# Kernel optimization log

Measured on AMD Instinct MI355X. Metric: run time of the kernel, lower is better.

The kernel has to match this reference:

```python
import jax, jax.numpy as jnp
import numpy as np

D = 256; NH = 8; HD = D // NH; FF = 1024; NLAYERS = 6
REG_MAX = 32; NBIN = REG_MAX + 1; NC = 80; KQ = 4
SPATIAL = [(80, 80), (40, 40), (20, 20)]; NPTS = [4, 4, 4]; SUMP = sum(NPTS)
LQ = 300; B = 16; OFFSET_SCALE = 0.5; UP = 0.5; REG_SCALE = 4.0
TOT = NH * SUMP


def _project_np():
    ub1 = abs(UP) * abs(REG_SCALE); ub2 = ub1 * 2
    step = (ub1 + 1.0) ** (2.0 / (REG_MAX - 2))
    left = [-(step ** i) + 1 for i in range(REG_MAX // 2 - 1, 0, -1)]
    right = [step ** i - 1 for i in range(1, REG_MAX // 2)]
    return np.array([-ub2] + left + [0.0] + right + [ub2], dtype=np.float32)

PROJ_NP = _project_np()  # [NBIN]


def layer_norm(x, g, b):
    mu = x.mean(-1, keepdims=True)
    var = ((x - mu) ** 2).mean(-1, keepdims=True)
    return (x - mu) * jax.lax.rsqrt(var + 1e-5) * g + b


def inv_sigmoid(x, eps=1e-5):
    x = jnp.clip(x, eps, 1.0 - eps)
    return jnp.log(x) - jnp.log1p(-x)


def mlp2(x, w1, b1, w2, b2):
    return jax.nn.silu(x @ w1 + b1) @ w2 + b2


def mlp3(x, w1, b1, w2, b2, w3, b3):
    return jax.nn.silu(jax.nn.silu(x @ w1 + b1) @ w2 + b2) @ w3 + b3


def grid_sample(img, grid):
    # bilinear, padding_mode='zeros', align_corners=False. img [N,C,H,W], grid [N,Hg,Wg,2] in [-1,1]
    N, C, H, W = img.shape
    gshape = grid.shape[1:3]
    x = (grid[..., 0] + 1.0) * (W * 0.5) - 0.5
    y = (grid[..., 1] + 1.0) * (H * 0.5) - 0.5
    x0f = jnp.floor(x); y0f = jnp.floor(y)
    wx = x - x0f; wy = y - y0f
    x0 = x0f.astype(jnp.int32); y0 = y0f.astype(jnp.int32)
    imgf = img.reshape(N, C, H * W)
    def tap(xi, yi, wt):
        valid = ((xi >= 0) & (xi < W) & (yi >= 0) & (yi < H)).astype(img.dtype)
        idx = jnp.clip(yi, 0, H - 1) * W + jnp.clip(xi, 0, W - 1)
        v = jnp.take_along_axis(imgf, idx.reshape(N, 1, -1), axis=2).reshape(N, C, gshape[0], gshape[1])
        return v * (valid * wt)[:, None]
    return (tap(x0, y0, (1 - wx) * (1 - wy)) + tap(x0 + 1, y0, wx * (1 - wy))
            + tap(x0, y0 + 1, (1 - wx) * wy) + tap(x0 + 1, y0 + 1, wx * wy))


def self_attention(q_in, k_in, v_in, qw, qb, kw, kb, vw, vb, ow, ob):
    q = (q_in @ qw + qb).reshape(B, LQ, NH, HD)
    k = (k_in @ kw + kb).reshape(B, LQ, NH, HD)
    v = (v_in @ vw + vb).reshape(B, LQ, NH, HD)
    a = jax.nn.softmax(jnp.einsum('bqhd,bkhd->bhqk', q, k) * (HD ** -0.5), -1)
    o = jnp.einsum('bhqk,bkhd->bqhd', a, v).reshape(B, LQ, D)
    return o @ ow + ob


def distance2bbox(points, distance):
    rs = abs(REG_SCALE); half = 0.5 * rs
    x1 = points[..., 0] - (half + distance[..., 0]) * (points[..., 2] / rs)
    y1 = points[..., 1] - (half + distance[..., 1]) * (points[..., 3] / rs)
    x2 = points[..., 0] + (half + distance[..., 2]) * (points[..., 2] / rs)
    y2 = points[..., 1] + (half + distance[..., 3]) * (points[..., 3] / rs)
    return jnp.stack([(x1 + x2) * 0.5, (y1 + y2) * 0.5, x2 - x1, y2 - y1], -1)


def lqe_head(scores, corners, w1, b1, w2, b2):
    prob = jax.nn.softmax(corners.reshape(B, LQ, 4, NBIN), -1)
    topk, _ = jax.lax.top_k(prob, KQ)                         # [B,LQ,4,KQ]
    stat = jnp.concatenate([topk, topk.mean(-1, keepdims=True)], -1)  # [B,LQ,4,KQ+1]
    return scores + mlp2(stat.reshape(B, LQ, 4 * (KQ + 1)), w1, b1, w2, b2)


def reference(target, ref_pts_unact, memory,
              sa_qw, sa_qb, sa_kw, sa_kb, sa_vw, sa_vb, sa_ow, sa_ob,
              n1_g, n1_b, off_w, off_b, aw_w, aw_b,
              gate_w, gate_b, gn_g, gn_b,
              ff1_w, ff1_b, ff2_w, ff2_b, n3_g, n3_b,
              bb_w1, bb_b1, bb_w2, bb_b2, bb_w3, bb_b3,
              sc_w, sc_b, lqe_w1, lqe_b1, lqe_w2, lqe_b2,
              qp_w1, qp_b1, qp_w2, qp_b2,
              pb_w1, pb_b1, pb_w2, pb_b2, pb_w3, pb_b3):
    project = jnp.asarray(PROJ_NP)
    # --- value prep: memory [B,S,D] -> per-level [B*NH, HD, h, w] ---
    val = memory.reshape(B, -1, NH, HD).transpose(0, 2, 3, 1).reshape(B * NH, HD, -1)
    splits = np.cumsum([h * w for h, w in SPATIAL])[:-1].tolist()
    value_lvls = [v.reshape(B * NH, HD, h, w)
                  for v, (h, w) in zip(jnp.split(val, splits, axis=2), SPATIAL)]
    nps = jnp.asarray(np.repeat(1.0 / np.array(NPTS, np.float32), NPTS))  # [SUMP]

    ref_pts = jax.nn.sigmoid(ref_pts_unact)
    output = target
    out_prev = jnp.zeros_like(target)
    corners_prev = jnp.zeros((B, LQ, 4 * NBIN), dtype=target.dtype)
    ref_init = ref_pts
    final_logits = final_bboxes = None

    for i in range(NLAYERS):
        qp = jnp.clip(mlp2(ref_pts, qp_w1, qp_b1, qp_w2, qp_b2), -10.0, 10.0)
        # self attention
        q = output + qp
        t2 = self_attention(q, q, output, sa_qw[i], sa_qb[i], sa_kw[i], sa_kb[i],
                            sa_vw[i], sa_vb[i], sa_ow[i], sa_ob[i])
        output = layer_norm(output + t2, n1_g[i], n1_b[i])
        # deformable cross attention
        qc = output + qp
        offs = (qc @ off_w[i] + off_b[i]).reshape(B, LQ, NH, SUMP, 2)
        attnw = jax.nn.softmax((qc @ aw_w[i] + aw_b[i]).reshape(B, LQ, NH, SUMP), -1)
        offset = offs * nps[:, None] * ref_pts[:, :, None, None, 2:] * OFFSET_SCALE
        locs = ref_pts[:, :, None, None, :2] + offset            # [B,LQ,NH,SUMP,2]
        grids = (2.0 * locs - 1.0).transpose(0, 2, 1, 3, 4).reshape(B * NH, LQ, SUMP, 2)
        p0 = 0; sampled = []
        for lvl in range(len(SPATIAL)):
            sampled.append(grid_sample(value_lvls[lvl], grids[:, :, p0:p0 + NPTS[lvl]]))
            p0 += NPTS[lvl]
        samp = jnp.concatenate(sampled, -1)                      # [B*NH, HD, LQ, SUMP]
        aw = attnw.transpose(0, 2, 1, 3).reshape(B * NH, 1, LQ, SUMP)
        t2 = (samp * aw).sum(-1).reshape(B, D, LQ).transpose(0, 2, 1)
        # gateway
        g12 = jax.nn.sigmoid(jnp.concatenate([output, t2], -1) @ gate_w[i] + gate_b[i])
        output = layer_norm(g12[..., :D] * output + g12[..., D:] * t2, gn_g[i], gn_b[i])
        # FFN
        t2 = jax.nn.relu(output @ ff1_w[i] + ff1_b[i]) @ ff2_w[i] + ff2_b[i]
        output = layer_norm(jnp.clip(output + t2, -65504.0, 65504.0), n3_g[i], n3_b[i])
        # FDR box refinement
        if i == 0:
            pre_bb = jax.nn.sigmoid(mlp3(output, pb_w1, pb_b1, pb_w2, pb_b2, pb_w3, pb_b3)
                                    + inv_sigmoid(ref_pts))
            ref_init = pre_bb
        corners = mlp3(output + out_prev, bb_w1[i], bb_b1[i], bb_w2[i], bb_b2[i],
                       bb_w3[i], bb_b3[i]) + corners_prev
        dist = jax.nn.softmax(corners.reshape(B, LQ, 4, NBIN), -1) @ project  # [B,LQ,4]
        inter = distance2bbox(ref_init, dist)
        if i == NLAYERS - 1:  # eval_idx
            scores = output @ sc_w[i] + sc_b[i]
            final_logits = lqe_head(scores, corners, lqe_w1[i], lqe_b1[i], lqe_w2[i], lqe_b2[i])
            final_bboxes = inter
        corners_prev = corners
        ref_pts = inter
        out_prev = output
    return jnp.concatenate([final_bboxes, final_logits], -1)  # [B, LQ, 4+NC]


def setup_inputs() -> dict:
    key = jax.random.key(0)
    cnt = [0]
    def rnd(shape, scale=0.02):
        cnt[0] += 1
        return jax.random.normal(jax.random.fold_in(key, cnt[0]), shape, dtype=jnp.float32) * scale
    S = sum(h * w for h, w in SPATIAL)
    L = NLAYERS
    return {
        'target': rnd((B, LQ, D), 1.0),
        'ref_pts_unact': rnd((B, LQ, 4), 1.0),
        'memory': rnd((B, S, D), 1.0),
        'sa_qw': rnd((L, D, D)), 'sa_qb': rnd((L, D)),
        'sa_kw': rnd((L, D, D)), 'sa_kb': rnd((L, D)),
        'sa_vw': rnd((L, D, D)), 'sa_vb': rnd((L, D)),
        'sa_ow': rnd((L, D, D)), 'sa_ob': rnd((L, D)),
        'n1_g': jnp.ones((L, D)), 'n1_b': jnp.zeros((L, D)),
        'off_w': rnd((L, D, TOT * 2)), 'off_b': rnd((L, TOT * 2)),
        'aw_w': rnd((L, D, TOT)), 'aw_b': rnd((L, TOT)),
        'gate_w': rnd((L, 2 * D, 2 * D)), 'gate_b': rnd((L, 2 * D)),
        'gn_g': jnp.ones((L, D)), 'gn_b': jnp.zeros((L, D)),
        'ff1_w': rnd((L, D, FF)), 'ff1_b': rnd((L, FF)),
        'ff2_w': rnd((L, FF, D)), 'ff2_b': rnd((L, D)),
        'n3_g': jnp.ones((L, D)), 'n3_b': jnp.zeros((L, D)),
        'bb_w1': rnd((L, D, D)), 'bb_b1': rnd((L, D)),
        'bb_w2': rnd((L, D, D)), 'bb_b2': rnd((L, D)),
        'bb_w3': rnd((L, D, 4 * NBIN)), 'bb_b3': rnd((L, 4 * NBIN)),
        'sc_w': rnd((L, D, NC)), 'sc_b': rnd((L, NC)),
        'lqe_w1': rnd((L, 4 * (KQ + 1), 64)), 'lqe_b1': rnd((L, 64)),
        'lqe_w2': rnd((L, 64, 1)), 'lqe_b2': rnd((L, 1)),
        'qp_w1': rnd((4, 2 * D)), 'qp_b1': rnd((2 * D,)),
        'qp_w2': rnd((2 * D, D)), 'qp_b2': rnd((D,)),
        'pb_w1': rnd((D, D)), 'pb_b1': rnd((D,)),
        'pb_w2': rnd((D, D)), 'pb_b2': rnd((D,)),
        'pb_w3': rnd((D, 4)), 'pb_b3': rnd((4,)),
    }
```

## Files before the change

### kernel.cpp

```cpp
#include <hip/hip_runtime.h>
#include <cstddef>
#include <cmath>
#include <utility>

#define B_ 16
#define LQ_ 300
#define D_ 256
#define NH_ 8
#define HD_ 32
#define FF_ 1024
#define NBIN_ 33
#define NC_ 80
#define SUMP_ 12
#define TOT_ (NH_*SUMP_)
#define STOT_ 8400
#define R_ (B_*LQ_)
#define NLAYERS_ 6

typedef short bf16x8 __attribute__((ext_vector_type(8)));
typedef float f32x4  __attribute__((ext_vector_type(4)));

static __device__ __forceinline__ short f2bf(float x) {
  union { float f; unsigned u; } v; v.f = x;
  unsigned r = v.u + 0x7fffu + ((v.u >> 16) & 1u);
  return (short)(r >> 16);
}
static __device__ __forceinline__ float bf2f(short s) {
  union { unsigned u; float f; } v; v.u = ((unsigned)(unsigned short)s) << 16; return v.f;
}

struct WJob { const float* src; short* dst; int K, N, tk, tn, L, ostride, blk0, pad; };
struct WJobs { WJob j[17]; int njobs; };

__launch_bounds__(256)
__global__ void wconv_all(WJobs P) {
  __shared__ float t[32][33];
  const int b = blockIdx.x;
  int ji = 0;
  for (int k = 1; k < P.njobs; ++k) ji = (b >= P.j[k].blk0) ? k : ji;
  const float* src = P.j[ji].src;
  short* dst = P.j[ji].dst;
  const int K = P.j[ji].K, N = P.j[ji].N, tk = P.j[ji].tk;
  int rel = b - P.j[ji].blk0;
  int per = tk * P.j[ji].tn;
  int l = rel / per; int r2 = rel - l * per;
  int tki = r2 % tk, tni = r2 / tk;
  const float* Wl = src + (size_t)l * K * N;
  short* Wtl = dst + (size_t)l * (size_t)P.j[ji].ostride;
  int k0 = tki * 32, n0 = tni * 32;
  int tr = threadIdx.x >> 5, tc = threadIdx.x & 31;
  #pragma unroll
  for (int i = 0; i < 4; ++i) {
    int k = k0 + tr + i * 8, n = n0 + tc;
    t[tr + i * 8][tc] = (k < K && n < N) ? Wl[(size_t)k * N + n] : 0.f;
  }
  __syncthreads();
  #pragma unroll
  for (int i = 0; i < 4; ++i) {
    int n = n0 + tr + i * 8, k = k0 + tc;
    if (n < N && k < K) Wtl[(size_t)n * K + k] = f2bf(t[tc][tr + i * 8]);
  }
}

__launch_bounds__(256)
__global__ void memconv_kernel(const float* __restrict__ mem, short* __restrict__ mb) {
  int gs = blockIdx.x * 4 + (threadIdx.x >> 6);
  int c  = (threadIdx.x & 63) * 4;
  int b = gs / STOT_, s = gs - b * STOT_;
  float4 v = *(const float4*)(mem + (size_t)gs * 256 + c);
  int h = c >> 5, cc = c & 31;
  short4 o; o.x = f2bf(v.x); o.y = f2bf(v.y); o.z = f2bf(v.z); o.w = f2bf(v.w);
  *(short4*)(mb + (((size_t)(b * 8 + h) * STOT_ + s) * 32) + cc) = o;
}

__launch_bounds__(256)
__global__ void misc_init(const float* __restrict__ target, const float* __restrict__ refu,
                          const float* __restrict__ qb, const float* __restrict__ kb,
                          const float* __restrict__ vb, const float* __restrict__ ob,
                          const float* __restrict__ ab,
                          float* __restrict__ output, short* __restrict__ outbf,
                          float* __restrict__ out_prev, float* __restrict__ cprev,
                          float* __restrict__ refcur, float* __restrict__ qkvb,
                          float* __restrict__ offawb) {
  int i = blockIdx.x * 256 + threadIdx.x;
  float4 z; z.x = 0.f; z.y = 0.f; z.z = 0.f; z.w = 0.f;
  if (i < R_ * 64) {
    float4 v = ((const float4*)target)[i];
    ((float4*)output)[i] = v;
    short4 s; s.x = f2bf(v.x); s.y = f2bf(v.y); s.z = f2bf(v.z); s.w = f2bf(v.w);
    ((short4*)outbf)[i] = s;
    ((float4*)out_prev)[i] = z;
  }
  if (i < R_ * 33) ((float4*)cprev)[i] = z;
  if (i < R_) {
    float4 r = ((const float4*)refu)[i];
    float4 o;
    o.x = 1.f / (1.f + __expf(-r.x)); o.y = 1.f / (1.f + __expf(-r.y));
    o.z = 1.f / (1.f + __expf(-r.z)); o.w = 1.f / (1.f + __expf(-r.w));
    ((float4*)refcur)[i] = o;
  }
  if (i < NLAYERS_ * 768) {
    int l = i / 768, c = i % 768;
    qkvb[i] = (c < 256) ? qb[l * 256 + c] : (c < 512) ? kb[l * 256 + c - 256]
                        : vb[l * 256 + c - 512];
  }
  if (i < NLAYERS_ * 288) {
    int l = i / 288, c = i % 288;
    offawb[i] = (c < 192) ? ob[l * 192 + c] : ab[l * 96 + c - 192];
  }
}

__launch_bounds__(256)
__global__ void qp_qkv(const float* __restrict__ ref, const float* __restrict__ W1,
                       const float* __restrict__ b1, const short* __restrict__ W2t,
                       const float* __restrict__ b2, const float* __restrict__ output,
                       const short* __restrict__ outbf,
                       const short* __restrict__ Qt, const float* __restrict__ qkvbias,
                       float* __restrict__ qpout, short* __restrict__ qkvout) {
  __shared__ short sh[16 * 520];
  __shared__ short oqs[16][264];
  const int m0 = blockIdx.x * 16;
  const int tid = threadIdx.x;
  for (int i = tid; i < 16 * 512; i += 256) {
    int r = i >> 9, n = i & 511;
    float4 rv = *(const float4*)(ref + (size_t)(m0 + r) * 4);
    float v = b1[n] + rv.x * W1[n] + rv.y * W1[512 + n] + rv.z * W1[1024 + n]
            + rv.w * W1[1536 + n];
    v = v / (1.f + __expf(-v));
    sh[r * 520 + n] = f2bf(v);
  }
  __syncthreads();
  const int wid = tid >> 6, lane = tid & 63;
  const int lr = lane & 15, lq = lane >> 4;
  {
    f32x4 acc[4];
    #pragma unroll
    for (int t = 0; t < 4; ++t) acc[t] = (f32x4){0.f, 0.f, 0.f, 0.f};
    #pragma unroll 4
    for (int k0 = 0; k0 < 512; k0 += 32) {
      bf16x8 a = *(const bf16x8*)&sh[lr * 520 + k0 + lq * 8];
      #pragma unroll
      for (int t = 0; t < 4; ++t) {
        bf16x8 w = *(const bf16x8*)(W2t + (size_t)(wid * 64 + t * 16 + lr) * 512 + k0 + lq * 8);
        acc[t] = __builtin_amdgcn_mfma_f32_16x16x32_bf16(a, w, acc[t], 0, 0, 0);
      }
    }
    #pragma unroll
    for (int t = 0; t < 4; ++t) {
      int col = wid * 64 + t * 16 + lr;
      float bv = b2[col];
      #pragma unroll
      for (int rr = 0; rr < 4; ++rr) {
        int rl = lq * 4 + rr;
        size_t idx = (size_t)(m0 + rl) * 256 + col;
        float v = fminf(fmaxf(acc[t][rr] + bv, -10.f), 10.f);
        qpout[idx] = v;
        oqs[rl][col] = f2bf(v + output[idx]);
      }
    }
  }
  __syncthreads();
  {
    f32x4 acc[12];
    #pragma unroll
    for (int t = 0; t < 12; ++t) acc[t] = (f32x4){0.f, 0.f, 0.f, 0.f};
    const int cbase = wid * 192;
    const short* obp = outbf + (size_t)(m0 + lr) * 256;
    #pragma unroll 2
    for (int k0 = 0; k0 < 256; k0 += 32) {
      bf16x8 a_oq = *(const bf16x8*)&oqs[lr][k0 + lq * 8];
      bf16x8 a_ob = *(const bf16x8*)(obp + k0 + lq * 8);
      #pragma unroll
      for (int t = 0; t < 12; ++t) {
        bf16x8 w = *(const bf16x8*)(Qt + (size_t)(cbase + t * 16 + lr) * 256 + k0 + lq * 8);
        acc[t] = __builtin_amdgcn_mfma_f32_16x16x32_bf16(
            (cbase + t * 16 < 512) ? a_oq : a_ob, w, acc[t], 0, 0, 0);
      }
    }
    #pragma unroll
    for (int t = 0; t < 12; ++t) {
      int colt = cbase + t * 16 + lr;
      float bv = qkvbias[colt];
      #pragma unroll
      for (int rr = 0; rr < 4; ++rr)
        qkvout[(size_t)(m0 + lq * 4 + rr) * 768 + colt] = f2bf(acc[t][rr] + bv);
    }
  }
}

__launch_bounds__(256)
__global__ void sow_ln_off(const short* __restrict__ A, const short* __restrict__ Wt,
                           const float* __restrict__ bias, const float* __restrict__ resid,
                           const float* __restrict__ gamma, const float* __restrict__ beta,
                           const float* __restrict__ qp,
                           const short* __restrict__ OWt, const float* __restrict__ ob,
                           float* __restrict__ outf, short* __restrict__ outbf,
                           float* __restrict__ offout) {
  __shared__ float ssum[16][4];
  __shared__ float ssq[16][4];
  __shared__ short oqs[16][264];
  const int m0 = blockIdx.x * 16;
  const int tid = threadIdx.x, wid = tid >> 6, lane = tid & 63;
  const int lr = lane & 15, lq = lane >> 4;
  const int arow = m0 + lr;
  const int cw = wid * 64;
  f32x4 acc[4];
  #pragma unroll
  for (int t = 0; t < 4; ++t) acc[t] = (f32x4){0.f, 0.f, 0.f, 0.f};
  #pragma unroll 4
  for (int k0 = 0; k0 < 256; k0 += 32) {
    bf16x8 a = *(const bf16x8*)(A + (size_t)arow * 256 + k0 + lq * 8);
    #pragma unroll
    for (int t = 0; t < 4; ++t) {
      bf16x8 w = *(const bf16x8*)(Wt + (size_t)(cw + t * 16 + lr) * 256 + k0 + lq * 8);
      acc[t] = __builtin_amdgcn_mfma_f32_16x16x32_bf16(a, w, acc[t], 0, 0, 0);
    }
  }
  float s[4] = {0.f, 0.f, 0.f, 0.f}, q[4] = {0.f, 0.f, 0.f, 0.f};
  #pragma unroll
  for (int t = 0; t < 4; ++t) {
    int col = cw + t * 16 + lr;
    float bv = bias[col];
    #pragma unroll
    for (int rr = 0; rr < 4; ++rr) {
      int rowg = m0 + lq * 4 + rr;
      float x = acc[t][rr] + bv + resid[(size_t)rowg * 256 + col];
      acc[t][rr] = x;
      s[rr] += x; q[rr] += x * x;
    }
  }
  #pragma unroll
  for (int m = 1; m < 16; m <<= 1)
    #pragma unroll
    for (int rr = 0; rr < 4; ++rr) { s[rr] += __shfl_xor(s[rr], m); q[rr] += __shfl_xor(q[rr], m); }
  if (lr == 0)
    #pragma unroll
    for (int rr = 0; rr < 4; ++rr) {
      ssum[lq * 4 + rr][wid] = s[rr];
      ssq[lq * 4 + rr][wid] = q[rr];
    }
  __syncthreads();
  float mu[4], rs[4];
  #pragma unroll
  for (int rr = 0; rr < 4; ++rr) {
    int rl = lq * 4 + rr;
    float sm = ssum[rl][0] + ssum[rl][1] + ssum[rl][2] + ssum[rl][3];
    float sq = ssq[rl][0] + ssq[rl][1] + ssq[rl][2] + ssq[rl][3];
    float m_ = sm * (1.f / 256.f);
    float var = sq * (1.f / 256.f) - m_ * m_;
    mu[rr] = m_; rs[rr] = rsqrtf(var + 1e-5f);
  }
  #pragma unroll
  for (int t = 0; t < 4; ++t) {
    int col = cw + t * 16 + lr;
    float g = gamma[col], be = beta[col];
    #pragma unroll
    for (int rr = 0; rr < 4; ++rr) {
      int rl = lq * 4 + rr;
      size_t idx = (size_t)(m0 + rl) * 256 + col;
      float v = (acc[t][rr] - mu[rr]) * rs[rr] * g + be;
      outf[idx] = v;
      outbf[idx] = f2bf(v);
      oqs[rl][col] = f2bf(v + qp[idx]);
    }
  }
  __syncthreads();
  f32x4 oacc[5];
  #pragma unroll
  for (int j = 0; j < 5; ++j) oacc[j] = (f32x4){0.f, 0.f, 0.f, 0.f};
  #pragma unroll 2
  for (int k0 = 0; k0 < 256; k0 += 32) {
    bf16x8 a = *(const bf16x8*)&oqs[lr][k0 + lq * 8];
    #pragma unroll
    for (int j = 0; j < 5; ++j) {
      int tile = wid + j * 4;
      int trow = (tile < 18) ? tile * 16 + lr : 0;
      bf16x8 w = *(const bf16x8*)(OWt + (size_t)trow * 256 + k0 + lq * 8);
      oacc[j] = __builtin_amdgcn_mfma_f32_16x16x32_bf16(a, w, oacc[j], 0, 0, 0);
    }
  }
  #pragma unroll
  for (int j = 0; j < 5; ++j) {
    int tile = wid + j * 4;
    if (tile >= 18) continue;
    int col = tile * 16 + lr;
    float bv = ob[col];
    #pragma unroll
    for (int rr = 0; rr < 4; ++rr)
      offout[(size_t)(m0 + lq * 4 + rr) * 288 + col] = oacc[j][rr] + bv;
  }
}

template<int SCORES>
__launch_bounds__(256)
__global__ void ffn_ln(const short* __restrict__ A, const short* __restrict__ W1t,
                       const float* __restrict__ b1, const short* __restrict__ W2t,
                       const float* __restrict__ b2, const float* __restrict__ resid,
                       const float* __restrict__ gamma, const float* __restrict__ beta,
                       float* __restrict__ prev, float* __restrict__ outf,
                       short* __restrict__ outbf, short* __restrict__ oqbf,
                       const short* __restrict__ SCt, const float* __restrict__ scb,
                       float* __restrict__ scoresOut) {
  __shared__ short hid[16][1032];
  __shared__ float ssum[16][4];
  __shared__ float ssq[16][4];
  const int m0 = blockIdx.x * 16;
  const int tid = threadIdx.x, wid = tid >> 6, lane = tid & 63;
  const int lr = lane & 15, lq = lane >> 4;
  const int arow = m0 + lr;
  {
    f32x4 acc[16];
    #pragma unroll
    for (int t = 0; t < 16; ++t) acc[t] = (f32x4){0.f, 0.f, 0.f, 0.f};
    #pragma unroll 2
    for (int k0 = 0; k0 < 256; k0 += 32) {
      bf16x8 a = *(const bf16x8*)(A + (size_t)arow * 256 + k0 + lq * 8);
      #pragma unroll
      for (int t = 0; t < 16; ++t) {
        bf16x8 w = *(const bf16x8*)(W1t + (size_t)(wid * 256 + t * 16 + lr) * 256 + k0 + lq * 8);
        acc[t] = __builtin_amdgcn_mfma_f32_16x16x32_bf16(a, w, acc[t], 0, 0, 0);
      }
    }
    #pragma unroll
    for (int t = 0; t < 16; ++t) {
      int col = wid * 256 + t * 16 + lr;
      float bv = b1[col];
      #pragma unroll
      for (int rr = 0; rr < 4; ++rr)
        hid[lq * 4 + rr][col] = f2bf(fmaxf(acc[t][rr] + bv, 0.f));
    }
  }
  __syncthreads();
  const int cw = wid * 64;
  f32x4 acc[4];
  #pragma unroll
  for (int t = 0; t < 4; ++t) acc[t] = (f32x4){0.f, 0.f, 0.f, 0.f};
  #pragma unroll 4
  for (int k0 = 0; k0 < 1024; k0 += 32) {
    bf16x8 a = *(const bf16x8*)&hid[lr][k0 + lq * 8];
    #pragma unroll
    for (int t = 0; t < 4; ++t) {
      bf16x8 w = *(const bf16x8*)(W2t + (size_t)(cw + t * 16 + lr) * 1024 + k0 + lq * 8);
      acc[t] = __builtin_amdgcn_mfma_f32_16x16x32_bf16(a, w, acc[t], 0, 0, 0);
    }
  }
  float s[4] = {0.f, 0.f, 0.f, 0.f}, q[4] = {0.f, 0.f, 0.f, 0.f};
  #pragma unroll
  for (int t = 0; t < 4; ++t) {
    int col = cw + t * 16 + lr;
    float bv = b2[col];
    #pragma unroll
    for (int rr = 0; rr < 4; ++rr) {
      int rowg = m0 + lq * 4 + rr;
      float x = acc[t][rr] + bv + resid[(size_t)rowg * 256 + col];
      x = fminf(fmaxf(x, -65504.f), 65504.f);
      acc[t][rr] = x;
      s[rr] += x; q[rr] += x * x;
    }
  }
  #pragma unroll
  for (int m = 1; m < 16; m <<= 1)
    #pragma unroll
    for (int rr = 0; rr < 4; ++rr) { s[rr] += __shfl_xor(s[rr], m); q[rr] += __shfl_xor(q[rr], m); }
  if (lr == 0)
    #pragma unroll
    for (int rr = 0; rr < 4; ++rr) {
      ssum[lq * 4 + rr][wid] = s[rr];
      ssq[lq * 4 + rr][wid] = q[rr];
    }
  __syncthreads();
  float mu[4], rs[4];
  #pragma unroll
  for (int rr = 0; rr < 4; ++rr) {
    int rl = lq * 4 + rr;
    float sm = ssum[rl][0] + ssum[rl][1] + ssum[rl][2] + ssum[rl][3];
    float sq = ssq[rl][0] + ssq[rl][1] + ssq[rl][2] + ssq[rl][3];
    float m_ = sm * (1.f / 256.f);
    float var = sq * (1.f / 256.f) - m_ * m_;
    mu[rr] = m_; rs[rr] = rsqrtf(var + 1e-5f);
  }
  #pragma unroll
  for (int t = 0; t < 4; ++t) {
    int col = cw + t * 16 + lr;
    float g = gamma[col], be = beta[col];
    #pragma unroll
    for (int rr = 0; rr < 4; ++rr) {
      int rl = lq * 4 + rr;
      size_t idx = (size_t)(m0 + rl) * 256 + col;
      float v = (acc[t][rr] - mu[rr]) * rs[rr] * g + be;
      outf[idx] = v;
      short vb = f2bf(v);
      outbf[idx] = vb;
      float po = prev[idx];
      oqbf[idx] = f2bf(v + po);
      prev[idx] = v;
      if (SCORES) hid[rl][col] = vb;
    }
  }
  if (SCORES) {
    __syncthreads();
    f32x4 sacc[2];
    sacc[0] = (f32x4){0.f, 0.f, 0.f, 0.f};
    sacc[1] = (f32x4){0.f, 0.f, 0.f, 0.f};
    #pragma unroll 2
    for (int k0 = 0; k0 < 256; k0 += 32) {
      bf16x8 a = *(const bf16x8*)&hid[lr][k0 + lq * 8];
      #pragma unroll
      for (int j = 0; j < 2; ++j) {
        int tile = wid + j * 4;
        int trow = (tile < 5) ? tile * 16 + lr : 0;
        bf16x8 w = *(const bf16x8*)(SCt + (size_t)trow * 256 + k0 + lq * 8);
        sacc[j] = __builtin_amdgcn_mfma_f32_16x16x32_bf16(a, w, sacc[j], 0, 0, 0);
      }
    }
    #pragma unroll
    for (int j = 0; j < 2; ++j) {
      int tile = wid + j * 4;
      if (tile >= 5) continue;
      int col = tile * 16 + lr;
      float bv = scb[col];
      #pragma unroll
      for (int rr = 0; rr < 4; ++rr)
        scoresOut[(size_t)(m0 + lq * 4 + rr) * 80 + col] = sacc[j][rr] + bv;
    }
  }
}

template<int LQE>
__launch_bounds__(256)
__global__ void fdr_kernel(const short* __restrict__ A,
                           const short* __restrict__ W1t, const float* __restrict__ b1,
                           const short* __restrict__ W2t, const float* __restrict__ b2,
                           const short* __restrict__ W3t, const float* __restrict__ b3,
                           const float* __restrict__ cprev, const float* __restrict__ refi,
                           float* __restrict__ ccur, float* __restrict__ refn,
                           const float* __restrict__ scores, const float* __restrict__ lw1,
                           const float* __restrict__ lb1, const float* __restrict__ lw2,
                           const float* __restrict__ lb2, float* __restrict__ outp) {
  __shared__ short h1[16][264];
  __shared__ short h2[16][264];
  __shared__ float cor[16][132];
  __shared__ float dstl[16][4];
  __shared__ float projs[33];
  __shared__ float statl[16][20];
  __shared__ float interb[16][4];
  __shared__ float lqes[16];
  const int m0 = blockIdx.x * 16;
  const int tid = threadIdx.x, wid = tid >> 6, lane = tid & 63;
  const int lr = lane & 15, lq = lane >> 4;
  if (tid < 33) {
    float v;
    if (tid == 0) v = -4.f;
    else if (tid == 32) v = 4.f;
    else if (tid == 16) v = 0.f;
    else if (tid < 16) v = 1.f - powf(3.f, (float)(16 - tid) * (1.f / 15.f));
    else v = powf(3.f, (float)(tid - 16) * (1.f / 15.f)) - 1.f;
    projs[tid] = v;
  }
  {
    f32x4 acc[4];
    #pragma unroll
    for (int t = 0; t < 4; ++t) acc[t] = (f32x4){0.f, 0.f, 0.f, 0.f};
    #pragma unroll 2
    for (int k0 = 0; k0 < 256; k0 += 32) {
      bf16x8 a = *(const bf16x8*)(A + (size_t)(m0 + lr) * 256 + k0 + lq * 8);
      #pragma unroll
      for (int t = 0; t < 4; ++t) {
        bf16x8 w = *(const bf16x8*)(W1t + (size_t)(wid * 64 + t * 16 + lr) * 256 + k0 + lq * 8);
        acc[t] = __builtin_amdgcn_mfma_f32_16x16x32_bf16(a, w, acc[t], 0, 0, 0);
      }
    }
    #pragma unroll
    for (int t = 0; t < 4; ++t) {
      int col = wid * 64 + t * 16 + lr;
      float bv = b1[col];
      #pragma unroll
      for (int rr = 0; rr < 4; ++rr) {
        float v = acc[t][rr] + bv;
        v = v / (1.f + __expf(-v));
        h1[lq * 4 + rr][col] = f2bf(v);
      }
    }
  }
  __syncthreads();
  {
    f32x4 acc[4];
    #pragma unroll
    for (int t = 0; t < 4; ++t) acc[t] = (f32x4){0.f, 0.f, 0.f, 0.f};
    #pragma unroll 2
    for (int k0 = 0; k0 < 256; k0 += 32) {
      bf16x8 a = *(const bf16x8*)&h1[lr][k0 + lq * 8];
      #pragma unroll
      for (int t = 0; t < 4; ++t) {
        bf16x8 w = *(const bf16x8*)(W2t + (size_t)(wid * 64 + t * 16 + lr) * 256 + k0 + lq * 8);
        acc[t] = __builtin_amdgcn_mfma_f32_16x16x32_bf16(a, w, acc[t], 0, 0, 0);
      }
    }
    #pragma unroll
    for (int t = 0; t < 4; ++t) {
      int col = wid * 64 + t * 16 + lr;
      float bv = b2[col];
      #pragma unroll
      for (int rr = 0; rr < 4; ++rr) {
        float v = acc[t][rr] + bv;
        v = v / (1.f + __expf(-v));
        h2[lq * 4 + rr][col] = f2bf(v);
      }
    }
  }
  __syncthreads();
  {
    f32x4 acc[3];
    int col[3], wr[3];
    #pragma unroll
    for (int j = 0; j < 3; ++j) {
      acc[j] = (f32x4){0.f, 0.f, 0.f, 0.f};
      col[j] = (wid + j * 4) * 16 + lr;
      wr[j] = (col[j] < 132) ? col[j] : 0;
    }
    #pragma unroll 2
    for (int k0 = 0; k0 < 256; k0 += 32) {
      bf16x8 a = *(const bf16x8*)&h2[lr][k0 + lq * 8];
      #pragma unroll
      for (int j = 0; j < 3; ++j) {
        bf16x8 w = *(const bf16x8*)(W3t + (size_t)wr[j] * 256 + k0 + lq * 8);
        acc[j] = __builtin_amdgcn_mfma_f32_16x16x32_bf16(a, w, acc[j], 0, 0, 0);
      }
    }
    #pragma unroll
    for (int j = 0; j < 3; ++j) {
      if (col[j] >= 132) continue;
      float bv = b3[col[j]];
      #pragma unroll
      for (int rr = 0; rr < 4; ++rr) {
        int rl = lq * 4 + rr, g = m0 + rl;
        float v = acc[j][rr] + bv + cprev[(size_t)g * 132 + col[j]];
        ccur[(size_t)g * 132 + col[j]] = v;
        cor[rl][col[j]] = v;
      }
    }
  }
  __syncthreads();
  if (tid < 64) {
    int r = tid >> 2, sd = tid & 3;
    const float* cp = &cor[r][sd * 33];
    float m = -1e30f;
    #pragma unroll
    for (int j = 0; j < 33; ++j) m = fmaxf(m, cp[j]);
    float t0 = -1e30f, t1 = -1e30f, t2v = -1e30f, t3 = -1e30f;
    float sum = 0.f, dot = 0.f;
    #pragma unroll
    for (int j = 0; j < 33; ++j) {
      float e = __expf(cp[j] - m);
      sum += e; dot += e * projs[j];
      if (LQE) {
        if (e > t0)      { t3 = t2v; t2v = t1; t1 = t0; t0 = e; }
        else if (e > t1) { t3 = t2v; t2v = t1; t1 = e; }
        else if (e > t2v){ t3 = t2v; t2v = e; }
        else if (e > t3) { t3 = e; }
      }
    }
    dstl[r][sd] = dot / sum;
    if (LQE) {
      float inv = 1.f / sum;
      float v0 = t0 * inv, v1 = t1 * inv, v2 = t2v * inv, v3 = t3 * inv;
      statl[r][sd * 5 + 0] = v0; statl[r][sd * 5 + 1] = v1;
      statl[r][sd * 5 + 2] = v2; statl[r][sd * 5 + 3] = v3;
      statl[r][sd * 5 + 4] = (v0 + v1 + v2 + v3) * 0.25f;
    }
  }
  __syncthreads();
  if (tid < 16) {
    int g = m0 + tid;
    float px = refi[g * 4], py = refi[g * 4 + 1];
    float qw = refi[g * 4 + 2] * 0.25f, qh = refi[g * 4 + 3] * 0.25f;
    float x1 = px - (2.f + dstl[tid][0]) * qw, y1 = py - (2.f + dstl[tid][1]) * qh;
    float x2 = px + (2.f + dstl[tid][2]) * qw, y2 = py + (2.f + dstl[tid][3]) * qh;
    float4 o; o.x = (x1 + x2) * 0.5f; o.y = (y1 + y2) * 0.5f; o.z = x2 - x1; o.w = y2 - y1;
    *(float4*)(refn + (size_t)g * 4) = o;
    if (LQE) { interb[tid][0] = o.x; interb[tid][1] = o.y; interb[tid][2] = o.z; interb[tid][3] = o.w; }
  }
  if (LQE) {
    #pragma unroll
    for (int it = 0; it < 4; ++it) {
      int row = wid * 4 + it;
      float sv = lb1[lane];
      #pragma unroll
      for (int i = 0; i < 20; ++i) sv += statl[row][i] * lw1[i * 64 + lane];
      float hv = sv / (1.f + __expf(-sv));
      float v = hv * lw2[lane];
      #pragma unroll
      for (int o = 32; o; o >>= 1) v += __shfl_xor(v, o);
      if (lane == 0) lqes[row] = v + lb2[0];
    }
    __syncthreads();
    for (int idx = tid; idx < 16 * 84; idx += 256) {
      int r = idx / 84, c = idx - r * 84;
      int g = m0 + r;
      outp[(size_t)g * 84 + c] = (c < 4) ? interb[r][c]
                                         : scores[(size_t)g * 80 + (c - 4)] + lqes[r];
    }
  }
}

__launch_bounds__(256)
__global__ void pb_fused(const short* __restrict__ A,
                         const short* __restrict__ W1t, const float* __restrict__ b1,
                         const short* __restrict__ W2t, const float* __restrict__ b2,
                         const short* __restrict__ W3t, const float* __restrict__ b3,
                         const float* __restrict__ refc, float* __restrict__ refinit) {
  __shared__ short h1[16][264];
  __shared__ short h2[16][264];
  const int m0 = blockIdx.x * 16;
  const int tid = threadIdx.x, wid = tid >> 6, lane = tid & 63;
  const int lr = lane & 15, lq = lane >> 4;
  {
    f32x4 acc[4];
    #pragma unroll
    for (int t = 0; t < 4; ++t) acc[t] = (f32x4){0.f, 0.f, 0.f, 0.f};
    #pragma unroll 2
    for (int k0 = 0; k0 < 256; k0 += 32) {
      bf16x8 a = *(const bf16x8*)(A + (size_t)(m0 + lr) * 256 + k0 + lq * 8);
      #pragma unroll
      for (int t = 0; t < 4; ++t) {
        bf16x8 w = *(const bf16x8*)(W1t + (size_t)(wid * 64 + t * 16 + lr) * 256 + k0 + lq * 8);
        acc[t] = __builtin_amdgcn_mfma_f32_16x16x32_bf16(a, w, acc[t], 0, 0, 0);
      }
    }
    #pragma unroll
    for (int t = 0; t < 4; ++t) {
      int col = wid * 64 + t * 16 + lr;
      float bv = b1[col];
      #pragma unroll
      for (int rr = 0; rr < 4; ++rr) {
        float v = acc[t][rr] + bv;
        v = v / (1.f + __expf(-v));
        h1[lq * 4 + rr][col] = f2bf(v);
      }
    }
  }
  __syncthreads();
  {
    f32x4 acc[4];
    #pragma unroll
    for (int t = 0; t < 4; ++t) acc[t] = (f32x4){0.f, 0.f, 0.f, 0.f};
    #pragma unroll 2
    for (int k0 = 0; k0 < 256; k0 += 32) {
      bf16x8 a = *(const bf16x8*)&h1[lr][k0 + lq * 8];
      #pragma unroll
      for (int t = 0; t < 4; ++t) {
        bf16x8 w = *(const bf16x8*)(W2t + (size_t)(wid * 64 + t * 16 + lr) * 256 + k0 + lq * 8);
        acc[t] = __builtin_amdgcn_mfma_f32_16x16x32_bf16(a, w, acc[t], 0, 0, 0);
      }
    }
    #pragma unroll
    for (int t = 0; t < 4; ++t) {
      int col = wid * 64 + t * 16 + lr;
      float bv = b2[col];
      #pragma unroll
      for (int rr = 0; rr < 4; ++rr) {
        float v = acc[t][rr] + bv;
        v = v / (1.f + __expf(-v));
        h2[lq * 4 + rr][col] = f2bf(v);
      }
    }
  }
  __syncthreads();
  if (wid == 0) {
    f32x4 acc = (f32x4){0.f, 0.f, 0.f, 0.f};
    const short* wp = W3t + (size_t)((lr < 4) ? lr : 0) * 256;
    #pragma unroll 2
    for (int k0 = 0; k0 < 256; k0 += 32) {
      bf16x8 a = *(const bf16x8*)&h2[lr][k0 + lq * 8];
      bf16x8 w = *(const bf16x8*)(wp + k0 + lq * 8);
      acc = __builtin_amdgcn_mfma_f32_16x16x32_bf16(a, w, acc, 0, 0, 0);
    }
    if (lr < 4) {
      float bv = b3[lr];
      #pragma unroll
      for (int rr = 0; rr < 4; ++rr) {
        int g = m0 + lq * 4 + rr;
        float pre = acc[rr] + bv;
        float x = fminf(fmaxf(refc[(size_t)g * 4 + lr], 1e-5f), 1.f - 1e-5f);
        float is = logf(x) - log1pf(-x);
        refinit[(size_t)g * 4 + lr] = 1.f / (1.f + __expf(-(pre + is)));
      }
    }
  }
}

__launch_bounds__(256)
__global__ void gate_ln(const short* __restrict__ Abf, const short* __restrict__ tbf,
                        const short* __restrict__ Wt, const float* __restrict__ bias,
                        const float* __restrict__ t2,
                        const float* __restrict__ gamma, const float* __restrict__ beta,
                        float* __restrict__ output, short* __restrict__ outbf) {
  __shared__ float sg[16][520];
  const int m0 = blockIdx.x * 16;
  const int tid = threadIdx.x, wid = tid >> 6, lane = tid & 63;
  const int lr = lane & 15, lq = lane >> 4;
  const int arow = m0 + lr;
  f32x4 acc[8];
  #pragma unroll
  for (int t = 0; t < 8; ++t) acc[t] = (f32x4){0.f, 0.f, 0.f, 0.f};
  #pragma unroll 2
  for (int k0 = 0; k0 < 512; k0 += 32) {
    const short* src = (k0 < 256) ? Abf : tbf;
    int ko = (k0 < 256) ? k0 : k0 - 256;
    bf16x8 a = *(const bf16x8*)(src + (size_t)arow * 256 + ko + lq * 8);
    #pragma unroll
    for (int t = 0; t < 8; ++t) {
      bf16x8 w = *(const bf16x8*)(Wt + (size_t)(wid * 128 + t * 16 + lr) * 512 + k0 + lq * 8);
      acc[t] = __builtin_amdgcn_mfma_f32_16x16x32_bf16(a, w, acc[t], 0, 0, 0);
    }
  }
  #pragma unroll
  for (int t = 0; t < 8; ++t) {
    int col = wid * 128 + t * 16 + lr;
    float bv = bias[col];
    #pragma unroll
    for (int rr = 0; rr < 4; ++rr) {
      int rl = lq * 4 + rr;
      sg[rl][col] = 1.f / (1.f + __expf(-(acc[t][rr] + bv)));
    }
  }
  __syncthreads();
  #pragma unroll
  for (int it = 0; it < 4; ++it) {
    int rl = wid + it * 4;
    int rowg = m0 + rl;
    int c = lane * 4;
    float4 o4 = *(const float4*)(output + (size_t)rowg * 256 + c);
    float4 t4 = *(const float4*)(t2 + (size_t)rowg * 256 + c);
    float4 g1 = *(const float4*)&sg[rl][c];
    float4 g2 = *(const float4*)&sg[rl][256 + c];
    float x0 = g1.x * o4.x + g2.x * t4.x;
    float x1 = g1.y * o4.y + g2.y * t4.y;
    float x2 = g1.z * o4.z + g2.z * t4.z;
    float x3 = g1.w * o4.w + g2.w * t4.w;
    float s = x0 + x1 + x2 + x3;
    float q = x0 * x0 + x1 * x1 + x2 * x2 + x3 * x3;
    #pragma unroll
    for (int o = 32; o; o >>= 1) { s += __shfl_xor(s, o); q += __shfl_xor(q, o); }
    float mu = s * (1.f / 256.f);
    float var = q * (1.f / 256.f) - mu * mu;
    float rs = rsqrtf(var + 1e-5f);
    float4 ga = *(const float4*)(gamma + c);
    float4 be = *(const float4*)(beta + c);
    float v0 = (x0 - mu) * rs * ga.x + be.x;
    float v1 = (x1 - mu) * rs * ga.y + be.y;
    float v2 = (x2 - mu) * rs * ga.z + be.z;
    float v3 = (x3 - mu) * rs * ga.w + be.w;
    float4 vo; vo.x = v0; vo.y = v1; vo.z = v2; vo.w = v3;
    *(float4*)(output + (size_t)rowg * 256 + c) = vo;
    short4 vs; vs.x = f2bf(v0); vs.y = f2bf(v1); vs.z = f2bf(v2); vs.w = f2bf(v3);
    *(short4*)(outbf + (size_t)rowg * 256 + c) = vs;
  }
}

__launch_bounds__(256)
__global__ void attn3_kernel(const short* __restrict__ qkv, short* __restrict__ O) {
  __shared__ short Kb[304][40];
  __shared__ short Vt[32][328];
  __shared__ short Pw[4][16][328];
  const int half = blockIdx.x & 1, bh = blockIdx.x >> 1;
  const int h = bh & 7, b = bh >> 3;
  const int tid = threadIdx.x;
  const short* QKVb = qkv + (size_t)b * LQ_ * 768;
  for (int idx = tid; idx < 304 * 4; idx += 256) {
    int row = idx >> 2, seg = (idx & 3) * 8;
    bf16x8 v = (row < 300) ? *(const bf16x8*)(QKVb + (size_t)row * 768 + 256 + h * 32 + seg)
                           : (bf16x8){0,0,0,0,0,0,0,0};
    *(bf16x8*)&Kb[row][seg] = v;
  }
  for (int idx = tid; idx < 300 * 4; idx += 256) {
    int row = idx >> 2, seg = (idx & 3) * 8;
    bf16x8 v = *(const bf16x8*)(QKVb + (size_t)row * 768 + 512 + h * 32 + seg);
    #pragma unroll
    for (int j = 0; j < 8; ++j) Vt[seg + j][row] = v[j];
  }
  for (int idx = tid; idx < 32 * 20; idx += 256) Vt[idx / 20][300 + idx % 20] = 0;
  for (int idx = tid; idx < 4 * 16 * 16; idx += 256)
    Pw[idx >> 8][(idx >> 4) & 15][304 + (idx & 15)] = 0;
  __syncthreads();

  const int wid = tid >> 6, lane = tid & 63;
  const int lr = lane & 15, lq = lane >> 4;
  short (*Pl)[328] = Pw[wid];
  const float scale = 0.17677669529663687f;

  for (int qt = wid; qt < 10; qt += 4) {
    const int q0 = half * 150 + qt * 16;
    int qrow = q0 + lr; if (qrow > 299) qrow = 299;
    bf16x8 af_q = *(const bf16x8*)(QKVb + (size_t)qrow * 768 + h * 32 + lq * 8);
    f32x4 s[19];
    #pragma unroll
    for (int t = 0; t < 19; ++t) {
      bf16x8 bk = *(const bf16x8*)&Kb[t * 16 + lr][lq * 8];
      s[t] = __builtin_amdgcn_mfma_f32_16x16x32_bf16(af_q, bk, (f32x4){0.f,0.f,0.f,0.f}, 0, 0, 0);
    }
    #pragma unroll
    for (int t = 0; t < 19; ++t)
      #pragma unroll
      for (int r = 0; r < 4; ++r) s[t][r] *= scale;
    if (lr >= 12) { s[18][0] = s[18][1] = s[18][2] = s[18][3] = -1e30f; }
    float l[4];
    #pragma unroll
    for (int r = 0; r < 4; ++r) {
      float mm = -1e30f;
      #pragma unroll
      for (int t = 0; t < 19; ++t) mm = fmaxf(mm, s[t][r]);
      #pragma unroll
      for (int x = 1; x < 16; x <<= 1) mm = fmaxf(mm, __shfl_xor(mm, x));
      float ll = 0.f;
      #pragma unroll
      for (int t = 0; t < 19; ++t) { float p = __expf(s[t][r] - mm); s[t][r] = p; ll += p; }
      #pragma unroll
      for (int x = 1; x < 16; x <<= 1) ll += __shfl_xor(ll, x);
      l[r] = ll;
    }
    #pragma unroll
    for (int t = 0; t < 19; ++t)
      #pragma unroll
      for (int r = 0; r < 4; ++r) Pl[lq * 4 + r][t * 16 + lr] = f2bf(s[t][r]);
    f32x4 o0 = (f32x4){0.f,0.f,0.f,0.f}, o1 = (f32x4){0.f,0.f,0.f,0.f};
    #pragma unroll
    for (int c = 0; c < 10; ++c) {
      bf16x8 ap = *(const bf16x8*)&Pl[lr][c * 32 + lq * 8];
      bf16x8 v0 = *(const bf16x8*)&Vt[lr][c * 32 + lq * 8];
      bf16x8 v1 = *(const bf16x8*)&Vt[16 + lr][c * 32 + lq * 8];
      o0 = __builtin_amdgcn_mfma_f32_16x16x32_bf16(ap, v0, o0, 0, 0, 0);
      o1 = __builtin_amdgcn_mfma_f32_16x16x32_bf16(ap, v1, o1, 0, 0, 0);
    }
    #pragma unroll
    for (int r = 0; r < 4; ++r) {
      int q = q0 + lq * 4 + r;
      if (q >= 300) continue;
      float inv = 1.f / l[r];
      size_t ob = (size_t)(b * LQ_ + q) * 256 + h * 32;
      O[ob + lr]      = f2bf(o0[r] * inv);
      O[ob + 16 + lr] = f2bf(o1[r] * inv);
    }
  }
}

template<int BF16MEM>
__launch_bounds__(256)
__global__ void deform_kernel(const void* __restrict__ memv, const float* __restrict__ offaw,
                              const float* __restrict__ refp,
                              float* __restrict__ t2, short* __restrict__ t2bf) {
  const int bi = blockIdx.x;
  const int row = (bi & 7) * 600 + (bi >> 3);
  const int b = row / LQ_;
  const int tid = threadIdx.x;
  const int h = tid >> 5, c = tid & 31;
  const float rx = refp[row * 4 + 0], ry = refp[row * 4 + 1];
  const float rw = refp[row * 4 + 2], rh = refp[row * 4 + 3];
  const float* awp = offaw + (size_t)row * 288 + 192 + h * SUMP_;
  float wv[SUMP_];
  float wmax = -1e30f;
  #pragma unroll
  for (int p = 0; p < SUMP_; ++p) { wv[p] = awp[p]; wmax = fmaxf(wmax, wv[p]); }
  float wsum = 0.f;
  #pragma unroll
  for (int p = 0; p < SUMP_; ++p) { wv[p] = __expf(wv[p] - wmax); wsum += wv[p]; }
  const float winv = 1.f / wsum;
  const float* op = offaw + (size_t)row * 288 + h * (SUMP_ * 2);
  const short* mb16 = BF16MEM ? ((const short*)memv + ((size_t)(b * 8 + h) * STOT_) * 32 + c) : nullptr;
  const float* mb32 = BF16MEM ? nullptr : ((const float*)memv + (size_t)b * STOT_ * 256 + h * 32 + c);
  float acc = 0.f;
  #pragma unroll
  for (int p = 0; p < SUMP_; ++p) {
    const int lvl = p >> 2;
    const int Wl = (lvl == 0) ? 80 : ((lvl == 1) ? 40 : 20);
    const int s0 = (lvl == 0) ? 0 : ((lvl == 1) ? 6400 : 8000);
    float lx = rx + op[2 * p]     * 0.125f * rw;
    float ly = ry + op[2 * p + 1] * 0.125f * rh;
    float x = lx * Wl - 0.5f, y = ly * Wl - 0.5f;
    float xf = floorf(x), yf = floorf(y);
    int x0 = (int)xf, y0 = (int)yf;
    float wx = x - xf, wy = y - yf;
    int x0c = min(max(x0, 0), Wl - 1), x1c = min(max(x0 + 1, 0), Wl - 1);
    int y0c = min(max(y0, 0), Wl - 1), y1c = min(max(y0 + 1, 0), Wl - 1);
    float wx0 = (x0 >= 0 && x0 < Wl) ? (1.f - wx) : 0.f;
    float wx1 = (x0 + 1 >= 0 && x0 + 1 < Wl) ? wx : 0.f;
    float wy0 = (y0 >= 0 && y0 < Wl) ? (1.f - wy) : 0.f;
    float wy1 = (y0 + 1 >= 0 && y0 + 1 < Wl) ? wy : 0.f;
    float v;
    if (BF16MEM) {
      const short* mb = mb16 + (size_t)s0 * 32;
      v = wx0 * wy0 * bf2f(mb[(size_t)(y0c * Wl + x0c) * 32])
        + wx1 * wy0 * bf2f(mb[(size_t)(y0c * Wl + x1c) * 32])
        + wx0 * wy1 * bf2f(mb[(size_t)(y1c * Wl + x0c) * 32])
        + wx1 * wy1 * bf2f(mb[(size_t)(y1c * Wl + x1c) * 32]);
    } else {
      const float* mb = mb32 + (size_t)s0 * 256;
      v = wx0 * wy0 * mb[(size_t)(y0c * Wl + x0c) * 256]
        + wx1 * wy0 * mb[(size_t)(y0c * Wl + x1c) * 256]
        + wx0 * wy1 * mb[(size_t)(y1c * Wl + x0c) * 256]
        + wx1 * wy1 * mb[(size_t)(y1c * Wl + x1c) * 256];
    }
    acc += wv[p] * winv * v;
  }
  size_t off = (size_t)row * D_ + h * HD_ + c;
  t2[off] = acc;
  t2bf[off] = f2bf(acc);
}

static inline dim3 egrid(int n) { return dim3((n + 255) / 256); }

extern "C" void kernel_launch(void* const* d_in, const int* in_sizes, int n_in,
                              void* d_out, int out_size, void* d_ws, size_t ws_size,
                              hipStream_t stream) {
  const float* target     = (const float*)d_in[0];
  const float* ref_unact  = (const float*)d_in[1];
  const float* memory     = (const float*)d_in[2];
  const float* sa_qw = (const float*)d_in[3];  const float* sa_qb = (const float*)d_in[4];
  const float* sa_kw = (const float*)d_in[5];  const float* sa_kb = (const float*)d_in[6];
  const float* sa_vw = (const float*)d_in[7];  const float* sa_vb = (const float*)d_in[8];
  const float* sa_ow = (const float*)d_in[9];  const float* sa_ob = (const float*)d_in[10];
  const float* n1_g  = (const float*)d_in[11]; const float* n1_b  = (const float*)d_in[12];
  const float* off_w = (const float*)d_in[13]; const float* off_b = (const float*)d_in[14];
  const float* aw_w  = (const float*)d_in[15]; const float* aw_b  = (const float*)d_in[16];
  const float* gate_w= (const float*)d_in[17]; const float* gate_b= (const float*)d_in[18];
  const float* gn_g  = (const float*)d_in[19]; const float* gn_b  = (const float*)d_in[20];
  const float* ff1_w = (const float*)d_in[21]; const float* ff1_b = (const float*)d_in[22];
  const float* ff2_w = (const float*)d_in[23]; const float* ff2_b = (const float*)d_in[24];
  const float* n3_g  = (const float*)d_in[25]; const float* n3_b  = (const float*)d_in[26];
  const float* bb_w1 = (const float*)d_in[27]; const float* bb_b1 = (const float*)d_in[28];
  const float* bb_w2 = (const float*)d_in[29]; const float* bb_b2 = (const float*)d_in[30];
  const float* bb_w3 = (const float*)d_in[31]; const float* bb_b3 = (const float*)d_in[32];
  const float* sc_w  = (const float*)d_in[33]; const float* sc_b  = (const float*)d_in[34];
  const float* lqe_w1= (const float*)d_in[35]; const float* lqe_b1= (const float*)d_in[36];
  const float* lqe_w2= (const float*)d_in[37]; const float* lqe_b2= (const float*)d_in[38];
  const float* qp_w1 = (const float*)d_in[39]; const float* qp_b1 = (const float*)d_in[40];
  const float* qp_w2 = (const float*)d_in[41]; const float* qp_b2 = (const float*)d_in[42];
  const float* pb_w1 = (const float*)d_in[43]; const float* pb_b1 = (const float*)d_in[44];
  const float* pb_w2 = (const float*)d_in[45]; const float* pb_b2 = (const float*)d_in[46];
  const float* pb_w3 = (const float*)d_in[47]; const float* pb_b3 = (const float*)d_in[48];
  float* out = (float*)d_out;

  float* ws = (float*)d_ws;
  size_t woff = 0;
  auto alloc = [&](size_t n) { float* p = ws + woff; woff += n; return p; };
  float* output   = alloc((size_t)R_ * D_);
  float* out_prev = alloc((size_t)R_ * D_);
  float* qp       = alloc((size_t)R_ * D_);
  float* t2       = alloc((size_t)R_ * D_);
  float* offawf   = alloc((size_t)R_ * 288);
  float* U        = alloc((size_t)R_ * 512);
  float* corners0 = alloc((size_t)R_ * 4 * NBIN_);
  float* corners1 = alloc((size_t)R_ * 4 * NBIN_);
  float* refA     = alloc((size_t)R_ * 4);
  float* refB     = alloc((size_t)R_ * 4);
  float* ref_init = alloc((size_t)R_ * 4);
  float* qkvb     = alloc((size_t)NLAYERS_ * 768);
  float* offawb   = alloc((size_t)NLAYERS_ * 288);

  short* sws = (short*)(ws + woff);
  size_t soff = 0;
  auto salloc = [&](size_t n) { short* p = sws + soff; soff += n; return p; };
  short* outbf = salloc((size_t)R_ * D_);
  short* oqbf  = salloc((size_t)R_ * D_);
  short* tbf   = salloc((size_t)R_ * D_);
  short* qp2t  = salloc((size_t)256 * 512);
  short* sqkvt = salloc((size_t)NLAYERS_ * 768 * 256);
  short* sowt  = salloc((size_t)NLAYERS_ * 256 * 256);
  short* soffawt = salloc((size_t)NLAYERS_ * 288 * 256);
  short* gatet = salloc((size_t)NLAYERS_ * 512 * 512);
  short* ff1t  = salloc((size_t)NLAYERS_ * 1024 * 256);
  short* ff2t  = salloc((size_t)NLAYERS_ * 256 * 1024);
  short* bb1t  = salloc((size_t)NLAYERS_ * 256 * 256);
  short* bb2t  = salloc((size_t)NLAYERS_ * 256 * 256);
  short* bb3t  = salloc((size_t)NLAYERS_ * 132 * 256);
  short* pb1t  = salloc((size_t)256 * 256);
  short* pb2t  = salloc((size_t)256 * 256);
  short* pb3t  = salloc((size_t)4 * 256);
  short* sct   = salloc((size_t)80 * 256);
  size_t base_bytes = woff * sizeof(float) + soff * sizeof(short);
  if (ws_size < base_bytes) return;
  const size_t memn = (size_t)B_ * STOT_ * 256;
  bool bf16mem = (ws_size >= base_bytes + memn * sizeof(short));
  short* membf = sws + soff;

  short* qkv    = (short*)U;
  float* scores = offawf;

  float* c_prev = corners0; float* c_cur = corners1;
  float* ref_cur = refA;    float* ref_nxt = refB;

  WJobs P; int nb = 0; int nj = 0;
  auto addj = [&](const float* s, short* d2, int K, int N, int L, int ostr) {
    P.j[nj].src = s; P.j[nj].dst = d2; P.j[nj].K = K; P.j[nj].N = N;
    P.j[nj].tk = (K + 31) / 32; P.j[nj].tn = (N + 31) / 32;
    P.j[nj].L = L; P.j[nj].ostride = ostr; P.j[nj].blk0 = nb; P.j[nj].pad = 0;
    nb += P.j[nj].tk * P.j[nj].tn * L; ++nj;
  };
  addj(qp_w2, qp2t, 512, 256, 1, 512 * 256);
  addj(sa_qw, sqkvt,               256, 256, NLAYERS_, 768 * 256);
  addj(sa_kw, sqkvt + 256 * 256,   256, 256, NLAYERS_, 768 * 256);
  addj(sa_vw, sqkvt + 512 * 256,   256, 256, NLAYERS_, 768 * 256);
  addj(sa_ow, sowt, 256, 256, NLAYERS_, 256 * 256);
  addj(off_w, soffawt,             256, 192, NLAYERS_, 288 * 256);
  addj(aw_w,  soffawt + 192 * 256, 256,  96, NLAYERS_, 288 * 256);
  addj(gate_w, gatet, 512, 512, NLAYERS_, 512 * 512);
  addj(ff1_w, ff1t, 256, 1024, NLAYERS_, 1024 * 256);
  addj(ff2_w, ff2t, 1024, 256, NLAYERS_, 256 * 1024);
  addj(bb_w1, bb1t, 256, 256, NLAYERS_, 256 * 256);
  addj(bb_w2, bb2t, 256, 256, NLAYERS_, 256 * 256);
  addj(bb_w3, bb3t, 256, 132, NLAYERS_, 132 * 256);
  addj(pb_w1, pb1t, 256, 256, 1, 256 * 256);
  addj(pb_w2, pb2t, 256, 256, 1, 256 * 256);
  addj(pb_w3, pb3t, 256, 4, 1, 4 * 256);
  addj(sc_w + (size_t)5 * D_ * NC_, sct, 256, 80, 1, 80 * 256);
  P.njobs = nj;
  wconv_all<<<dim3(nb), 256, 0, stream>>>(P);
  if (bf16mem)
    memconv_kernel<<<dim3(B_ * STOT_ / 4), 256, 0, stream>>>(memory, membf);

  misc_init<<<egrid(R_ * 64), 256, 0, stream>>>(target, ref_unact,
      sa_qb, sa_kb, sa_vb, off_b, aw_b,
      output, outbf, out_prev, c_prev, ref_cur, qkvb, offawb);

  for (int i = 0; i < NLAYERS_; ++i) {
    qp_qkv<<<dim3(300), 256, 0, stream>>>(ref_cur, qp_w1, qp_b1, qp2t, qp_b2,
                                          output, outbf,
                                          sqkvt + (size_t)i * 768 * 256,
                                          qkvb + (size_t)i * 768, qp, qkv);
    attn3_kernel<<<dim3(B_ * NH_ * 2), 256, 0, stream>>>(qkv, tbf);
    sow_ln_off<<<dim3(300), 256, 0, stream>>>(
        tbf, sowt + (size_t)i * 65536, sa_ob + (size_t)i * D_, output,
        n1_g + (size_t)i * D_, n1_b + (size_t)i * D_, qp,
        soffawt + (size_t)i * 288 * 256, offawb + (size_t)i * 288,
        output, outbf, offawf);

    if (bf16mem)
      deform_kernel<1><<<dim3(R_), 256, 0, stream>>>(membf, offawf, ref_cur, t2, tbf);
    else
      deform_kernel<0><<<dim3(R_), 256, 0, stream>>>(memory, offawf, ref_cur, t2, tbf);

    gate_ln<<<dim3(300), 256, 0, stream>>>(outbf, tbf, gatet + (size_t)i * 262144,
                                           gate_b + (size_t)i * 512, t2,
                                           gn_g + (size_t)i * D_, gn_b + (size_t)i * D_,
                                           output, outbf);

    if (i < NLAYERS_ - 1)
      ffn_ln<0><<<dim3(300), 256, 0, stream>>>(outbf, ff1t + (size_t)i * 262144,
          ff1_b + (size_t)i * FF_, ff2t + (size_t)i * 262144, ff2_b + (size_t)i * D_,
          output, n3_g + (size_t)i * D_, n3_b + (size_t)i * D_,
          out_prev, output, outbf, oqbf, nullptr, nullptr, nullptr);
    else
      ffn_ln<1><<<dim3(300), 256, 0, stream>>>(outbf, ff1t + (size_t)i * 262144,
          ff1_b + (size_t)i * FF_, ff2t + (size_t)i * 262144, ff2_b + (size_t)i * D_,
          output, n3_g + (size_t)i * D_, n3_b + (size_t)i * D_,
          out_prev, output, outbf, oqbf, sct, sc_b + (size_t)5 * NC_, scores);

    if (i == 0)
      pb_fused<<<dim3(300), 256, 0, stream>>>(outbf, pb1t, pb_b1, pb2t, pb_b2,
                                              pb3t, pb_b3, ref_cur, ref_init);
    if (i < NLAYERS_ - 1) {
      fdr_kernel<0><<<dim3(300), 256, 0, stream>>>(oqbf,
          bb1t + (size_t)i * 65536, bb_b1 + (size_t)i * D_,
          bb2t + (size_t)i * 65536, bb_b2 + (size_t)i * D_,
          bb3t + (size_t)i * 33792, bb_b3 + (size_t)i * 4 * NBIN_,
          c_prev, ref_init, c_cur, ref_nxt,
          nullptr, nullptr, nullptr, nullptr, nullptr, nullptr);
      std::swap(c_prev, c_cur);
      std::swap(ref_cur, ref_nxt);
    } else {
      fdr_kernel<1><<<dim3(300), 256, 0, stream>>>(oqbf,
          bb1t + (size_t)i * 65536, bb_b1 + (size_t)i * D_,
          bb2t + (size_t)i * 65536, bb_b2 + (size_t)i * D_,
          bb3t + (size_t)i * 33792, bb_b3 + (size_t)i * 4 * NBIN_,
          c_prev, ref_init, c_cur, ref_nxt,
          scores, lqe_w1 + (size_t)5 * 20 * 64, lqe_b1 + (size_t)5 * 64,
          lqe_w2 + (size_t)5 * 64, lqe_b2 + (size_t)5, out);
    }
  }
}
```

Before: 1.893 ms.

## Double block size to 512 threads in row-tile MFMA kernels, halving per-wave tiles

Launches the 16-row GEMM+LayerNorm kernels (qp_qkv, sow_ln_off, gate_ln, ffn_ln, fdr_kernel, pb_fused) with 8 waves instead of 4. Each wave now owns half as many output column tiles, and the LN partial-sum reductions and row loops are re-indexed for 8 waves. With only 300 blocks on a large GPU, the aim is more waves per CU to hide latency and fewer accumulator registers per wave. The cost is that some waves idle in the narrow tail GEMMs (scores, offsets), and there are more threads per barrier. Parts of fdr_kernel not shown may still assume 4 waves.

Measured after the change: 1.885 ms. No clear change (-0.5%).

```diff
diff --git a/kernel.cpp b/kernel.cpp
--- a/kernel.cpp
+++ b/kernel.cpp
@@ -110,7 +110,7 @@
   }
 }
 
-__launch_bounds__(256)
+__launch_bounds__(512)
 __global__ void qp_qkv(const float* __restrict__ ref, const float* __restrict__ W1,
                        const float* __restrict__ b1, const short* __restrict__ W2t,
                        const float* __restrict__ b2, const float* __restrict__ output,
@@ -121,7 +121,7 @@
   __shared__ short oqs[16][264];
   const int m0 = blockIdx.x * 16;
   const int tid = threadIdx.x;
-  for (int i = tid; i < 16 * 512; i += 256) {
+  for (int i = tid; i < 16 * 512; i += 512) {
     int r = i >> 9, n = i & 511;
     float4 rv = *(const float4*)(ref + (size_t)(m0 + r) * 4);
     float v = b1[n] + rv.x * W1[n] + rv.y * W1[512 + n] + rv.z * W1[1024 + n]
@@ -133,21 +133,21 @@
   const int wid = tid >> 6, lane = tid & 63;
   const int lr = lane & 15, lq = lane >> 4;
   {
-    f32x4 acc[4];
-    #pragma unroll
-    for (int t = 0; t < 4; ++t) acc[t] = (f32x4){0.f, 0.f, 0.f, 0.f};
+    f32x4 acc[2];
+    acc[0] = (f32x4){0.f, 0.f, 0.f, 0.f};
+    acc[1] = (f32x4){0.f, 0.f, 0.f, 0.f};
     #pragma unroll 4
     for (int k0 = 0; k0 < 512; k0 += 32) {
       bf16x8 a = *(const bf16x8*)&sh[lr * 520 + k0 + lq * 8];
       #pragma unroll
-      for (int t = 0; t < 4; ++t) {
-        bf16x8 w = *(const bf16x8*)(W2t + (size_t)(wid * 64 + t * 16 + lr) * 512 + k0 + lq * 8);
+      for (int t = 0; t < 2; ++t) {
+        bf16x8 w = *(const bf16x8*)(W2t + (size_t)(wid * 32 + t * 16 + lr) * 512 + k0 + lq * 8);
         acc[t] = __builtin_amdgcn_mfma_f32_16x16x32_bf16(a, w, acc[t], 0, 0, 0);
       }
     }
     #pragma unroll
-    for (int t = 0; t < 4; ++t) {
-      int col = wid * 64 + t * 16 + lr;
+    for (int t = 0; t < 2; ++t) {
+      int col = wid * 32 + t * 16 + lr;
       float bv = b2[col];
       #pragma unroll
       for (int rr = 0; rr < 4; ++rr) {
@@ -161,24 +161,24 @@
   }
   __syncthreads();
   {
-    f32x4 acc[12];
-    #pragma unroll
-    for (int t = 0; t < 12; ++t) acc[t] = (f32x4){0.f, 0.f, 0.f, 0.f};
-    const int cbase = wid * 192;
+    f32x4 acc[6];
+    #pragma unroll
+    for (int t = 0; t < 6; ++t) acc[t] = (f32x4){0.f, 0.f, 0.f, 0.f};
+    const int cbase = wid * 96;
     const short* obp = outbf + (size_t)(m0 + lr) * 256;
     #pragma unroll 2
     for (int k0 = 0; k0 < 256; k0 += 32) {
       bf16x8 a_oq = *(const bf16x8*)&oqs[lr][k0 + lq * 8];
       bf16x8 a_ob = *(const bf16x8*)(obp + k0 + lq * 8);
       #pragma unroll
-      for (int t = 0; t < 12; ++t) {
+      for (int t = 0; t < 6; ++t) {
         bf16x8 w = *(const bf16x8*)(Qt + (size_t)(cbase + t * 16 + lr) * 256 + k0 + lq * 8);
         acc[t] = __builtin_amdgcn_mfma_f32_16x16x32_bf16(
             (cbase + t * 16 < 512) ? a_oq : a_ob, w, acc[t], 0, 0, 0);
       }
     }
     #pragma unroll
-    for (int t = 0; t < 12; ++t) {
+    for (int t = 0; t < 6; ++t) {
       int colt = cbase + t * 16 + lr;
       float bv = qkvbias[colt];
       #pragma unroll
@@ -188,7 +188,7 @@
   }
 }
 
-__launch_bounds__(256)
+__launch_bounds__(512)
 __global__ void sow_ln_off(const short* __restrict__ A, const short* __restrict__ Wt,
                            const float* __restrict__ bias, const float* __restrict__ resid,
                            const float* __restrict__ gamma, const float* __restrict__ beta,
@@ -196,29 +196,29 @@
                            const short* __restrict__ OWt, const float* __restrict__ ob,
                            float* __restrict__ outf, short* __restrict__ outbf,
                            float* __restrict__ offout) {
-  __shared__ float ssum[16][4];
-  __shared__ float ssq[16][4];
+  __shared__ float ssum[16][8];
+  __shared__ float ssq[16][8];
   __shared__ short oqs[16][264];
   const int m0 = blockIdx.x * 16;
   const int tid = threadIdx.x, wid = tid >> 6, lane = tid & 63;
   const int lr = lane & 15, lq = lane >> 4;
   const int arow = m0 + lr;
-  const int cw = wid * 64;
-  f32x4 acc[4];
-  #pragma unroll
-  for (int t = 0; t < 4; ++t) acc[t] = (f32x4){0.f, 0.f, 0.f, 0.f};
+  const int cw = wid * 32;
+  f32x4 acc[2];
+  acc[0] = (f32x4){0.f, 0.f, 0.f, 0.f};
+  acc[1] = (f32x4){0.f, 0.f, 0.f, 0.f};
   #pragma unroll 4
   for (int k0 = 0; k0 < 256; k0 += 32) {
     bf16x8 a = *(const bf16x8*)(A + (size_t)arow * 256 + k0 + lq * 8);
     #pragma unroll
-    for (int t = 0; t < 4; ++t) {
+    for (int t = 0; t < 2; ++t) {
       bf16x8 w = *(const bf16x8*)(Wt + (size_t)(cw + t * 16 + lr) * 256 + k0 + lq * 8);
       acc[t] = __builtin_amdgcn_mfma_f32_16x16x32_bf16(a, w, acc[t], 0, 0, 0);
     }
   }
   float s[4] = {0.f, 0.f, 0.f, 0.f}, q[4] = {0.f, 0.f, 0.f, 0.f};
   #pragma unroll
-  for (int t = 0; t < 4; ++t) {
+  for (int t = 0; t < 2; ++t) {
     int col = cw + t * 16 + lr;
     float bv = bias[col];
     #pragma unroll
@@ -244,14 +244,15 @@
   #pragma unroll
   for (int rr = 0; rr < 4; ++rr) {
     int rl = lq * 4 + rr;
-    float sm = ssum[rl][0] + ssum[rl][1] + ssum[rl][2] + ssum[rl][3];
-    float sq = ssq[rl][0] + ssq[rl][1] + ssq[rl][2] + ssq[rl][3];
+    float sm = 0.f, sq = 0.f;
+    #pragma unroll
+    for (int w8 = 0; w8 < 8; ++w8) { sm += ssum[rl][w8]; sq += ssq[rl][w8]; }
     float m_ = sm * (1.f / 256.f);
     float var = sq * (1.f / 256.f) - m_ * m_;
     mu[rr] = m_; rs[rr] = rsqrtf(var + 1e-5f);
   }
   #pragma unroll
-  for (int t = 0; t < 4; ++t) {
+  for (int t = 0; t < 2; ++t) {
     int col = cw + t * 16 + lr;
     float g = gamma[col], be = beta[col];
     #pragma unroll
@@ -265,23 +266,23 @@
     }
   }
   __syncthreads();
-  f32x4 oacc[5];
-  #pragma unroll
-  for (int j = 0; j < 5; ++j) oacc[j] = (f32x4){0.f, 0.f, 0.f, 0.f};
+  f32x4 oacc[3];
+  #pragma unroll
+  for (int j = 0; j < 3; ++j) oacc[j] = (f32x4){0.f, 0.f, 0.f, 0.f};
   #pragma unroll 2
   for (int k0 = 0; k0 < 256; k0 += 32) {
     bf16x8 a = *(const bf16x8*)&oqs[lr][k0 + lq * 8];
     #pragma unroll
-    for (int j = 0; j < 5; ++j) {
-      int tile = wid + j * 4;
+    for (int j = 0; j < 3; ++j) {
+      int tile = wid + j * 8;
       int trow = (tile < 18) ? tile * 16 + lr : 0;
       bf16x8 w = *(const bf16x8*)(OWt + (size_t)trow * 256 + k0 + lq * 8);
       oacc[j] = __builtin_amdgcn_mfma_f32_16x16x32_bf16(a, w, oacc[j], 0, 0, 0);
     }
   }
   #pragma unroll
-  for (int j = 0; j < 5; ++j) {
-    int tile = wid + j * 4;
+  for (int j = 0; j < 3; ++j) {
+    int tile = wid + j * 8;
     if (tile >= 18) continue;
     int col = tile * 16 + lr;
     float bv = ob[col];
@@ -292,7 +293,7 @@
 }
 
 template<int SCORES>
-__launch_bounds__(256)
+__launch_bounds__(512)
 __global__ void ffn_ln(const short* __restrict__ A, const short* __restrict__ W1t,
                        const float* __restrict__ b1, const short* __restrict__ W2t,
                        const float* __restrict__ b2, const float* __restrict__ resid,
@@ -302,28 +303,28 @@
                        const short* __restrict__ SCt, const float* __restrict__ scb,
                        float* __restrict__ scoresOut) {
   __shared__ short hid[16][1032];
-  __shared__ float ssum[16][4];
-  __shared__ float ssq[16][4];
+  __shared__ float ssum[16][8];
+  __shared__ float ssq[16][8];
   const int m0 = blockIdx.x * 16;
   const int tid = threadIdx.x, wid = tid >> 6, lane = tid & 63;
   const int lr = lane & 15, lq = lane >> 4;
   const int arow = m0 + lr;
   {
-    f32x4 acc[16];
-    #pragma unroll
-    for (int t = 0; t < 16; ++t) acc[t] = (f32x4){0.f, 0.f, 0.f, 0.f};
+    f32x4 acc[8];
+    #pragma unroll
+    for (int t = 0; t < 8; ++t) acc[t] = (f32x4){0.f, 0.f, 0.f, 0.f};
     #pragma unroll 2
     for (int k0 = 0; k0 < 256; k0 += 32) {
       bf16x8 a = *(const bf16x8*)(A + (size_t)arow * 256 + k0 + lq * 8);
       #pragma unroll
-      for (int t = 0; t < 16; ++t) {
-        bf16x8 w = *(const bf16x8*)(W1t + (size_t)(wid * 256 + t * 16 + lr) * 256 + k0 + lq * 8);
+      for (int t = 0; t < 8; ++t) {
+        bf16x8 w = *(const bf16x8*)(W1t + (size_t)(wid * 128 + t * 16 + lr) * 256 + k0 + lq * 8);
         acc[t] = __builtin_amdgcn_mfma_f32_16x16x32_bf16(a, w, acc[t], 0, 0, 0);
       }
     }
     #pragma unroll
-    for (int t = 0; t < 16; ++t) {
-      int col = wid * 256 + t * 16 + lr;
+    for (int t = 0; t < 8; ++t) {
+      int col = wid * 128 + t * 16 + lr;
       float bv = b1[col];
       #pragma unroll
       for (int rr = 0; rr < 4; ++rr)
@@ -331,22 +332,22 @@
     }
   }
   __syncthreads();
-  const int cw = wid * 64;
-  f32x4 acc[4];
-  #pragma unroll
-  for (int t = 0; t < 4; ++t) acc[t] = (f32x4){0.f, 0.f, 0.f, 0.f};
+  const int cw = wid * 32;
+  f32x4 acc[2];
+  acc[0] = (f32x4){0.f, 0.f, 0.f, 0.f};
+  acc[1] = (f32x4){0.f, 0.f, 0.f, 0.f};
   #pragma unroll 4
   for (int k0 = 0; k0 < 1024; k0 += 32) {
     bf16x8 a = *(const bf16x8*)&hid[lr][k0 + lq * 8];
     #pragma unroll
-    for (int t = 0; t < 4; ++t) {
+    for (int t = 0; t < 2; ++t) {
       bf16x8 w = *(const bf16x8*)(W2t + (size_t)(cw + t * 16 + lr) * 1024 + k0 + lq * 8);
       acc[t] = __builtin_amdgcn_mfma_f32_16x16x32_bf16(a, w, acc[t], 0, 0, 0);
     }
   }
   float s[4] = {0.f, 0.f, 0.f, 0.f}, q[4] = {0.f, 0.f, 0.f, 0.f};
   #pragma unroll
-  for (int t = 0; t < 4; ++t) {
+  for (int t = 0; t < 2; ++t) {
     int col = cw + t * 16 + lr;
     float bv = b2[col];
     #pragma unroll
@@ -373,14 +374,15 @@
   #pragma unroll
   for (int rr = 0; rr < 4; ++rr) {
     int rl = lq * 4 + rr;
-    float sm = ssum[rl][0] + ssum[rl][1] + ssum[rl][2] + ssum[rl][3];
-    float sq = ssq[rl][0] + ssq[rl][1] + ssq[rl][2] + ssq[rl][3];
+    float sm = 0.f, sq = 0.f;
+    #pragma unroll
+    for (int w8 = 0; w8 < 8; ++w8) { sm += ssum[rl][w8]; sq += ssq[rl][w8]; }
     float m_ = sm * (1.f / 256.f);
     float var = sq * (1.f / 256.f) - m_ * m_;
     mu[rr] = m_; rs[rr] = rsqrtf(var + 1e-5f);
   }
   #pragma unroll
-  for (int t = 0; t < 4; ++t) {
+  for (int t = 0; t < 2; ++t) {
     int col = cw + t * 16 + lr;
     float g = gamma[col], be = beta[col];
     #pragma unroll
@@ -399,35 +401,26 @@
   }
   if (SCORES) {
     __syncthreads();
-    f32x4 sacc[2];
-    sacc[0] = (f32x4){0.f, 0.f, 0.f, 0.f};
-    sacc[1] = (f32x4){0.f, 0.f, 0.f, 0.f};
+    f32x4 sacc = (f32x4){0.f, 0.f, 0.f, 0.f};
+    int trow = (wid < 5) ? wid * 16 + lr : 0;
     #pragma unroll 2
     for (int k0 = 0; k0 < 256; k0 += 32) {
       bf16x8 a = *(const bf16x8*)&hid[lr][k0 + lq * 8];
-      #pragma unroll
-      for (int j = 0; j < 2; ++j) {
-        int tile = wid + j * 4;
-        int trow = (tile < 5) ? tile * 16 + lr : 0;
-        bf16x8 w = *(const bf16x8*)(SCt + (size_t)trow * 256 + k0 + lq * 8);
-        sacc[j] = __builtin_amdgcn_mfma_f32_16x16x32_bf16(a, w, sacc[j], 0, 0, 0);
-      }
-    }
-    #pragma unroll
-    for (int j = 0; j < 2; ++j) {
-      int tile = wid + j * 4;
-      if (tile >= 5) continue;
-      int col = tile * 16 + lr;
+      bf16x8 w = *(const bf16x8*)(SCt + (size_t)trow * 256 + k0 + lq * 8);
+      sacc = __builtin_amdgcn_mfma_f32_16x16x32_bf16(a, w, sacc, 0, 0, 0);
+    }
+    if (wid < 5) {
+      int col = wid * 16 + lr;
       float bv = scb[col];
       #pragma unroll
       for (int rr = 0; rr < 4; ++rr)
-        scoresOut[(size_t)(m0 + lq * 4 + rr) * 80 + col] = sacc[j][rr] + bv;
+        scoresOut[(size_t)(m0 + lq * 4 + rr) * 80 + col] = sacc[rr] + bv;
     }
   }
 }
 
 template<int LQE>
-__launch_bounds__(256)
+__launch_bounds__(512)
 __global__ void fdr_kernel(const short* __restrict__ A,
                            const short* __restrict__ W1t, const float* __restrict__ b1,
                            const short* __restrict__ W2t, const float* __restrict__ b2,
@@ -458,21 +451,21 @@
     projs[tid] = v;
   }
   {
-    f32x4 acc[4];
-    #pragma unroll
-    for (int t = 0; t < 4; ++t) acc[t] = (f32x4){0.f, 0.f, 0.f, 0.f};
+    f32x4 acc[2];
+    acc[0] = (f32x4){0.f, 0.f, 0.f, 0.f};
+    acc[1] = (f32x4){0.f, 0.f, 0.f, 0.f};
     #pragma unroll 2
     for (int k0 = 0; k0 < 256; k0 += 32) {
       bf16x8 a = *(const bf16x8*)(A + (size_t)(m0 + lr) * 256 + k0 + lq * 8);
       #pragma unroll
-      for (int t = 0; t < 4; ++t) {
-        bf16x8 w = *(const bf16x8*)(W1t + (size_t)(wid * 64 + t * 16 + lr) * 256 + k0 + lq * 8);
+      for (int t = 0; t < 2; ++t) {
+        bf16x8 w = *(const bf16x8*)(W1t + (size_t)(wid * 32 + t * 16 + lr) * 256 + k0 + lq * 8);
         acc[t] = __builtin_amdgcn_mfma_f32_16x16x32_bf16(a, w, acc[t], 0, 0, 0);
       }
     }
     #pragma unroll
-    for (int t = 0; t < 4; ++t) {
-      int col = wid * 64 + t * 16 + lr;
+    for (int t = 0; t < 2; ++t) {
+      int col = wid * 32 + t * 16 + lr;
       float bv = b1[col];
       #pragma unroll
       for (int rr = 0; rr < 4; ++rr) {
@@ -484,21 +477,21 @@
   }
   __syncthreads();
   {
-    f32x4 acc[4];
-    #pragma unroll
-    for (int t = 0; t < 4; ++t) acc[t] = (f32x4){0.f, 0.f, 0.f, 0.f};
+    f32x4 acc[2];
+    acc[0] = (f32x4){0.f, 0.f, 0.f, 0.f};
+    acc[1] = (f32x4){0.f, 0.f, 0.f, 0.f};
     #pragma unroll 2
     for (int k0 = 0; k0 < 256; k0 += 32) {
       bf16x8 a = *(const bf16x8*)&h1[lr][k0 + lq * 8];
       #pragma unroll
-      for (int t = 0; t < 4; ++t) {
-        bf16x8 w = *(const bf16x8*)(W2t + (size_t)(wid * 64 + t * 16 + lr) * 256 + k0 + lq * 8);
+      for (int t = 0; t < 2; ++t) {
+        bf16x8 w = *(const bf16x8*)(W2t + (size_t)(wid * 32 + t * 16 + lr) * 256 + k0 + lq * 8);
         acc[t] = __builtin_amdgcn_mfma_f32_16x16x32_bf16(a, w, acc[t], 0, 0, 0);
       }
     }
     #pragma unroll
-    for (int t = 0; t < 4; ++t) {
-      int col = wid * 64 + t * 16 + lr;
+    for (int t = 0; t < 2; ++t) {
+      int col = wid * 32 + t * 16 + lr;
       float bv = b2[col];
       #pragma unroll
       for (int rr = 0; rr < 4; ++rr) {
@@ -510,25 +503,25 @@
   }
   __syncthreads();
   {
-    f32x4 acc[3];
-    int col[3], wr[3];
-    #pragma unroll
-    for (int j = 0; j < 3; ++j) {
+    f32x4 acc[2];
+    int col[2], wr[2];
+    #pragma unroll
+    for (int j = 0; j < 2; ++j) {
       acc[j] = (f32x4){0.f, 0.f, 0.f, 0.f};
-      col[j] = (wid + j * 4) * 16 + lr;
+      col[j] = (wid + j * 8) * 16 + lr;
       wr[j] = (col[j] < 132) ? col[j] : 0;
     }
     #pragma unroll 2
     for (int k0 = 0; k0 < 256; k0 += 32) {
       bf16x8 a = *(const bf16x8*)&h2[lr][k0 + lq * 8];
       #pragma unroll
-      for (int j = 0; j < 3; ++j) {
+      for (int j = 0; j < 2; ++j) {
         bf16x8 w = *(const bf16x8*)(W3t + (size_t)wr[j] * 256 + k0 + lq * 8);
         acc[j] = __builtin_amdgcn_mfma_f32_16x16x32_bf16(a, w, acc[j], 0, 0, 0);
       }
     }
     #pragma unroll
-    for (int j = 0; j < 3; ++j) {
+    for (int j = 0; j < 2; ++j) {
       if (col[j] >= 132) continue;
       float bv = b3[col[j]];
       #pragma unroll
@@ -582,8 +575,8 @@
   }
   if (LQE) {
     #pragma unroll
-    for (int it = 0; it < 4; ++it) {
-      int row = wid * 4 + it;
+    for (int it = 0; it < 2; ++it) {
+      int row = wid * 2 + it;
       float sv = lb1[lane];
       #pragma unroll
       for (int i = 0; i < 20; ++i) sv += statl[row][i] * lw1[i * 64 + lane];
@@ -594,7 +587,7 @@
       if (lane == 0) lqes[row] = v + lb2[0];
     }
     __syncthreads();
-    for (int idx = tid; idx < 16 * 84; idx += 256) {
+    for (int idx = tid; idx < 16 * 84; idx += 512) {
       int r = idx / 84, c = idx - r * 84;
       int g = m0 + r;
       outp[(size_t)g * 84 + c] = (c < 4) ? interb[r][c]
@@ -603,7 +596,7 @@
   }
 }
 
-__launch_bounds__(256)
+__launch_bounds__(512)
 __global__ void pb_fused(const short* __restrict__ A,
                          const short* __restrict__ W1t, const float* __restrict__ b1,
                          const short* __restrict__ W2t, const float* __restrict__ b2,
@@ -615,21 +608,21 @@
   const int tid = threadIdx.x, wid = tid >> 6, lane = tid & 63;
   const int lr = lane & 15, lq = lane >> 4;
   {
-    f32x4 acc[4];
-    #pragma unroll
-    for (int t = 0; t < 4; ++t) acc[t] = (f32x4){0.f, 0.f, 0.f, 0.f};
+    f32x4 acc[2];
+    acc[0] = (f32x4){0.f, 0.f, 0.f, 0.f};
+    acc[1] = (f32x4){0.f, 0.f, 0.f, 0.f};
     #pragma unroll 2
     for (int k0 = 0; k0 < 256; k0 += 32) {
       bf16x8 a = *(const bf16x8*)(A + (size_t)(m0 + lr) * 256 + k0 + lq * 8);
       #pragma unroll
-      for (int t = 0; t < 4; ++t) {
-        bf16x8 w = *(const bf16x8*)(W1t + (size_t)(wid * 64 + t * 16 + lr) * 256 + k0 + lq * 8);
+      for (int t = 0; t < 2; ++t) {
+        bf16x8 w = *(const bf16x8*)(W1t + (size_t)(wid * 32 + t * 16 + lr) * 256 + k0 + lq * 8);
         acc[t] = __builtin_amdgcn_mfma_f32_16x16x32_bf16(a, w, acc[t], 0, 0, 0);
       }
     }
     #pragma unroll
-    for (int t = 0; t < 4; ++t) {
-      int col = wid * 64 + t * 16 + lr;
+    for (int t = 0; t < 2; ++t) {
+      int col = wid * 32 + t * 16 + lr;
       float bv = b1[col];
       #pragma unroll
       for (int rr = 0; rr < 4; ++rr) {
@@ -641,21 +634,21 @@
   }
   __syncthreads();
   {
-    f32x4 acc[4];
-    #pragma unroll
-    for (int t = 0; t < 4; ++t) acc[t] = (f32x4){0.f, 0.f, 0.f, 0.f};
+    f32x4 acc[2];
+    acc[0] = (f32x4){0.f, 0.f, 0.f, 0.f};
+    acc[1] = (f32x4){0.f, 0.f, 0.f, 0.f};
     #pragma unroll 2
     for (int k0 = 0; k0 < 256; k0 += 32) {
       bf16x8 a = *(const bf16x8*)&h1[lr][k0 + lq * 8];
       #pragma unroll
-      for (int t = 0; t < 4; ++t) {
-        bf16x8 w = *(const bf16x8*)(W2t + (size_t)(wid * 64 + t * 16 + lr) * 256 + k0 + lq * 8);
+      for (int t = 0; t < 2; ++t) {
+        bf16x8 w = *(const bf16x8*)(W2t + (size_t)(wid * 32 + t * 16 + lr) * 256 + k0 + lq * 8);
         acc[t] = __builtin_amdgcn_mfma_f32_16x16x32_bf16(a, w, acc[t], 0, 0, 0);
       }
     }
     #pragma unroll
-    for (int t = 0; t < 4; ++t) {
-      int col = wid * 64 + t * 16 + lr;
+    for (int t = 0; t < 2; ++t) {
+      int col = wid * 32 + t * 16 + lr;
       float bv = b2[col];
       #pragma unroll
       for (int rr = 0; rr < 4; ++rr) {
@@ -689,7 +682,7 @@
   }
 }
 
-__launch_bounds__(256)
+__launch_bounds__(512)
 __global__ void gate_ln(const short* __restrict__ Abf, const short* __restrict__ tbf,
                         const short* __restrict__ Wt, const float* __restrict__ bias,
                         const float* __restrict__ t2,
@@ -700,23 +693,23 @@
   const int tid = threadIdx.x, wid = tid >> 6, lane = tid & 63;
   const int lr = lane & 15, lq = lane >> 4;
   const int arow = m0 + lr;
-  f32x4 acc[8];
-  #pragma unroll
-  for (int t = 0; t < 8; ++t) acc[t] = (f32x4){0.f, 0.f, 0.f, 0.f};
+  f32x4 acc[4];
+  #pragma unroll
+  for (int t = 0; t < 4; ++t) acc[t] = (f32x4){0.f, 0.f, 0.f, 0.f};
   #pragma unroll 2
   for (int k0 = 0; k0 < 512; k0 += 32) {
     const short* src = (k0 < 256) ? Abf : tbf;
     int ko = (k0 < 256) ? k0 : k0 - 256;
     bf16x8 a = *(const bf16x8*)(src + (size_t)arow * 256 + ko + lq * 8);
     #pragma unroll
-    for (int t = 0; t < 8; ++t) {
-      bf16x8 w = *(const bf16x8*)(Wt + (size_t)(wid * 128 + t * 16 + lr) * 512 + k0 + lq * 8);
+    for (int t = 0; t < 4; ++t) {
+      bf16x8 w = *(const bf16x8*)(Wt + (size_t)(wid * 64 + t * 16 + lr) * 512 + k0 + lq * 8);
       acc[t] = __builtin_amdgcn_mfma_f32_16x16x32_bf16(a, w, acc[t], 0, 0, 0);
     }
   }
   #pragma unroll
-  for (int t = 0; t < 8; ++t) {
-    int col = wid * 128 + t * 16 + lr;
+  for (int t = 0; t < 4; ++t) {
+    int col = wid * 64 + t * 16 + lr;
     float bv = bias[col];
     #pragma unroll
     for (int rr = 0; rr < 4; ++rr) {
@@ -726,8 +719,8 @@
   }
   __syncthreads();
   #pragma unroll
-  for (int it = 0; it < 4; ++it) {
-    int rl = wid + it * 4;
+  for (int it = 0; it < 2; ++it) {
+    int rl = wid + it * 8;
     int rowg = m0 + rl;
     int c = lane * 4;
     float4 o4 = *(const float4*)(output + (size_t)rowg * 256 + c);
@@ -1023,12 +1016,12 @@
       output, outbf, out_prev, c_prev, ref_cur, qkvb, offawb);
 
   for (int i = 0; i < NLAYERS_; ++i) {
-    qp_qkv<<<dim3(300), 256, 0, stream>>>(ref_cur, qp_w1, qp_b1, qp2t, qp_b2,
+    qp_qkv<<<dim3(300), 512, 0, stream>>>(ref_cur, qp_w1, qp_b1, qp2t, qp_b2,
                                           output, outbf,
                                           sqkvt + (size_t)i * 768 * 256,
                                           qkvb + (size_t)i * 768, qp, qkv);
     attn3_kernel<<<dim3(B_ * NH_ * 2), 256, 0, stream>>>(qkv, tbf);
-    sow_ln_off<<<dim3(300), 256, 0, stream>>>(
+    sow_ln_off<<<dim3(300), 512, 0, stream>>>(
         tbf, sowt + (size_t)i * 65536, sa_ob + (size_t)i * D_, output,
         n1_g + (size_t)i * D_, n1_b + (size_t)i * D_, qp,
         soffawt + (size_t)i * 288 * 256, offawb + (size_t)i * 288,
@@ -1039,27 +1032,27 @@
     else
       deform_kernel<0><<<dim3(R_), 256, 0, stream>>>(memory, offawf, ref_cur, t2, tbf);
 
-    gate_ln<<<dim3(300), 256, 0, stream>>>(outbf, tbf, gatet + (size_t)i * 262144,
+    gate_ln<<<dim3(300), 512, 0, stream>>>(outbf, tbf, gatet + (size_t)i * 262144,
                                            gate_b + (size_t)i * 512, t2,
                                            gn_g + (size_t)i * D_, gn_b + (size_t)i * D_,
                                            output, outbf);
 
     if (i < NLAYERS_ - 1)
-      ffn_ln<0><<<dim3(300), 256, 0, stream>>>(outbf, ff1t + (size_t)i * 262144,
+      ffn_ln<0><<<dim3(300), 512, 0, stream>>>(outbf, ff1t + (size_t)i * 262144,
           ff1_b + (size_t)i * FF_, ff2t + (size_t)i * 262144, ff2_b + (size_t)i * D_,
           output, n3_g + (size_t)i * D_, n3_b + (size_t)i * D_,
           out_prev, output, outbf, oqbf, nullptr, nullptr, nullptr);
     else
-      ffn_ln<1><<<dim3(300), 256, 0, stream>>>(outbf, ff1t + (size_t)i * 262144,
+      ffn_ln<1><<<dim3(300), 512, 0, stream>>>(outbf, ff1t + (size_t)i * 262144,
           ff1_b + (size_t)i * FF_, ff2t + (size_t)i * 262144, ff2_b + (size_t)i * D_,
           output, n3_g + (size_t)i * D_, n3_b + (size_t)i * D_,
           out_prev, output, outbf, oqbf, sct, sc_b + (size_t)5 * NC_, scores);
 
     if (i == 0)
-      pb_fused<<<dim3(300), 256, 0, stream>>>(outbf, pb1t, pb_b1, pb2t, pb_b2,
+      pb_fused<<<dim3(300), 512, 0, stream>>>(outbf, pb1t, pb_b1, pb2t, pb_b2,
                                               pb3t, pb_b3, ref_cur, ref_init);
     if (i < NLAYERS_ - 1) {
-      fdr_kernel<0><<<dim3(300), 256, 0, stream>>>(oqbf,
+      fdr_kernel<0><<<dim3(300), 512, 0, stream>>>(oqbf,
           bb1t + (size_t)i * 65536, bb_b1 + (size_t)i * D_,
           bb2t + (size_t)i * 65536, bb_b2 + (size_t)i * D_,
           bb3t + (size_t)i * 33792, bb_b3 + (size_t)i * 4 * NBIN_,
@@ -1068,7 +1061,7 @@
       std::swap(c_prev, c_cur);
       std::swap(ref_cur, ref_nxt);
     } else {
-      fdr_kernel<1><<<dim3(300), 256, 0, stream>>>(oqbf,
+      fdr_kernel<1><<<dim3(300), 512, 0, stream>>>(oqbf,
           bb1t + (size_t)i * 65536, bb_b1 + (size_t)i * D_,
           bb2t + (size_t)i * 65536, bb_b2 + (size_t)i * D_,
           bb3t + (size_t)i * 33792, bb_b3 + (size_t)i * 4 * NBIN_,
```
